# Kernel tuning notes

Measured on AMD Instinct MI355X. Metric: run time of the kernel, lower is better.

## Reference

```python
import jax, jax.numpy as jnp
import numpy as np

NG, ND = 50000, 10000          # gene / disease node counts
IN, HID = 64, 128              # in_feats / hidden_feats
EGG, EGD, EDG = 800000, 300000, 300000
EPS = 1e-5


def setup_inputs() -> dict:
    key = jax.random.key(0)
    ks = jax.random.split(key, 18)
    s = 0.05
    return {
        "xg": jax.random.normal(ks[0], (NG, IN), jnp.float32),
        "xd": jax.random.normal(ks[1], (ND, IN), jnp.float32),
        "Wn0": jax.random.normal(ks[2], (3, IN, HID), jnp.float32) * s,
        "Ws0": jax.random.normal(ks[3], (3, IN, HID), jnp.float32) * s,
        "b0": jnp.zeros((3, HID), jnp.float32),
        "Wn1": jax.random.normal(ks[4], (3, HID, HID), jnp.float32) * s,
        "Ws1": jax.random.normal(ks[5], (3, HID, HID), jnp.float32) * s,
        "b1": jnp.zeros((3, HID), jnp.float32),
        "bng": jnp.ones((2, 2, HID), jnp.float32),   # [layer, ntype, HID]
        "bnb": jnp.zeros((2, 2, HID), jnp.float32),
        "Wp": jax.random.normal(ks[6], (2, HID, IN), jnp.float32) * s,
        "bp": jnp.zeros((2, IN), jnp.float32),
        "gg_src": jax.random.randint(ks[7], (EGG,), 0, NG, jnp.int32),
        "gg_dst": jax.random.randint(ks[8], (EGG,), 0, NG, jnp.int32),
        "gd_src": jax.random.randint(ks[9], (EGD,), 0, NG, jnp.int32),
        "gd_dst": jax.random.randint(ks[10], (EGD,), 0, ND, jnp.int32),
        "dg_src": jax.random.randint(ks[11], (EDG,), 0, ND, jnp.int32),
        "dg_dst": jax.random.randint(ks[12], (EDG,), 0, NG, jnp.int32),
    }


def _seg_mean(h_src, src_idx, dst_idx, num_dst):
    # gather source features along edges, mean-reduce onto destinations
    msg = h_src[src_idx]                                         # [E, D]
    ssum = jax.ops.segment_sum(msg, dst_idx, num_segments=num_dst)
    deg = jax.ops.segment_sum(jnp.ones((dst_idx.shape[0], 1), h_src.dtype),
                              dst_idx, num_segments=num_dst)
    return ssum / jnp.maximum(deg, 1.0)                          # zero-degree -> 0


def _sage(h_src, h_dst, src_idx, dst_idx, num_dst, Wn, Ws, b):
    # DGL SAGEConv(mean): fc_neigh(mean_neigh) + fc_self(h_dst) + bias
    m = _seg_mean(h_src, src_idx, dst_idx, num_dst)
    return m @ Wn + h_dst @ Ws + b


def _bn_relu(x, g, b):
    # BatchNorm1d in training mode (batch statistics) followed by ReLU
    mu = x.mean(axis=0)
    var = x.var(axis=0)
    return jax.nn.relu((x - mu) * jax.lax.rsqrt(var + EPS) * g + b)


def _hetero_layer(hg, hd, Wn, Ws, b, idx):
    gg_s, gg_d, gd_s, gd_d, dg_s, dg_d = idx
    # HeteroGraphConv aggregate='sum' across relations per destination type
    out_g = (_sage(hg, hg, gg_s, gg_d, NG, Wn[0], Ws[0], b[0]) +
             _sage(hd, hg, dg_s, dg_d, NG, Wn[2], Ws[2], b[2]))
    out_d = _sage(hg, hd, gd_s, gd_d, ND, Wn[1], Ws[1], b[1])
    return out_g, out_d


def reference(xg, xd, Wn0, Ws0, b0, Wn1, Ws1, b1, bng, bnb, Wp, bp,
              gg_src, gg_dst, gd_src, gd_dst, dg_src, dg_dst):
    idx = (gg_src, gg_dst, gd_src, gd_dst, dg_src, dg_dst)
    # layer 0
    hg, hd = _hetero_layer(xg, xd, Wn0, Ws0, b0, idx)
    hg = _bn_relu(hg, bng[0, 0], bnb[0, 0])
    hd = _bn_relu(hd, bng[0, 1], bnb[0, 1])
    # layer 1
    hg, hd = _hetero_layer(hg, hd, Wn1, Ws1, b1, idx)
    hg = _bn_relu(hg, bng[1, 0], bnb[1, 0])
    hd = _bn_relu(hd, bng[1, 1], bnb[1, 1])
    # final per-type projection back to in_feats
    out_g = hg @ Wp[0] + bp[0]
    out_d = hd @ Wp[1] + bp[1]
    return out_g, out_d
```

## Files before the change

### kernel.cpp

```cpp
#include <hip/hip_runtime.h>

typedef unsigned short u16;
typedef __attribute__((ext_vector_type(8))) short bf16x8;
typedef __attribute__((ext_vector_type(4))) float f32x4;

__device__ __forceinline__ float BF(u16 u) { return __uint_as_float(((unsigned)u) << 16); }
__device__ __forceinline__ float BLO(unsigned p) { return __uint_as_float(p << 16); }
__device__ __forceinline__ float BHI(unsigned p) { return __uint_as_float(p & 0xffff0000u); }
__device__ __forceinline__ u16 FBF(float f) {
    unsigned u = __float_as_uint(f);
    u += 0x7FFFu + ((u >> 16) & 1u);
    return (u16)(u >> 16);
}
__device__ __forceinline__ unsigned PK2(float a, float b) {
    return (unsigned)FBF(a) | ((unsigned)FBF(b) << 16);
}
__device__ __forceinline__ float LD(const void* p, long i, int isf) {
    if (isf) return ((const float*)p)[i];
    return BF(((const u16*)p)[i]);
}

__global__ void HeteroGNN_78426102825755_kernel() {}

__global__ void hk_fill16(u16* p, long n, u16 v) {
    long i = (long)blockIdx.x * 256 + threadIdx.x;
    if (i < n) p[i] = v;
}
__global__ void hk_zeroi(int* p, int n) {
    int i = blockIdx.x * 256 + threadIdx.x;
    if (i < n) p[i] = 0;
}

__global__ void hk_detect(const void* x, int* flag) {
    __shared__ int cnt;
    if (threadIdx.x == 0) cnt = 0;
    __syncthreads();
    unsigned w = ((const unsigned*)x)[threadIdx.x];
    int e = (w >> 7) & 0xFF;
    int pl = (e >= 0x68 && e <= 0x92) ? 1 : 0;
    atomicAdd(&cnt, pl);
    __syncthreads();
    if (threadIdx.x == 0) flag[0] = (cnt >= 192) ? 0 : 1;
}

__device__ __forceinline__ void wprep_one(const void* W, int K, int ncol, int persh, int ksh,
                                          unsigned* dst, int i, int isf) {
    int mslice = i >> persh;
    int d2 = i & ((1 << persh) - 1);
    int mat = mslice >> ksh;
    int ks = mslice & ((1 << ksh) - 1);
    int ct = d2 >> 8; int rr = d2 & 255; int ln = rr >> 2; int j2 = rr & 3;
    int k1 = ks * 32 + ((ln >> 4) * 8 + 2 * j2);
    int n = ct * 16 + (ln & 15);
    long e = (long)mat * K * ncol + (long)k1 * ncol + n;
    dst[i] = PK2(LD(W, e, isf), LD(W, e + ncol, isf));
}
__device__ __forceinline__ void wsum_one(const void* W, int K, unsigned* dst, int i, int isf) {
    int ks = i >> 11; int d2 = i & 2047;
    int ct = d2 >> 8; int rr = d2 & 255; int ln = rr >> 2; int j2 = rr & 3;
    int k1 = ks * 32 + ((ln >> 4) * 8 + 2 * j2);
    int n = ct * 16 + (ln & 15);
    long e = (long)k1 * 128 + n;
    long e2 = e + (long)2 * K * 128;
    dst[i] = PK2(LD(W, e, isf) + LD(W, e2, isf), LD(W, e + 128, isf) + LD(W, e2 + 128, isf));
}

__global__ void hk_prep2(const void* Wn0, const void* Ws0, const void* Wn1, const void* Ws1,
                         unsigned* f0n, unsigned* f0s, unsigned* f1n, unsigned* f1s,
                         unsigned* f0sum, unsigned* f1sum,
                         const void* xg, const void* xd, long n0, long n1,
                         u16* og, u16* od, int* ncur, int Tn, int B1,
                         const int* dflag) {
    int isf = dflag[0];
    int b = blockIdx.x, t = threadIdx.x;
    if (b < 48)       { wprep_one(Wn0, 64, 128, 11, 1, f0n, b * 256 + t, isf); return; }
    if (b < 96)       { wprep_one(Ws0, 64, 128, 11, 1, f0s, (b - 48) * 256 + t, isf); return; }
    if (b < 192)      { wprep_one(Wn1, 128, 128, 11, 2, f1n, (b - 96) * 256 + t, isf); return; }
    if (b < 288)      { wprep_one(Ws1, 128, 128, 11, 2, f1s, (b - 192) * 256 + t, isf); return; }
    if (b < 304)      { wsum_one(Ws0, 64, f0sum, (b - 288) * 256 + t, isf); return; }
    if (b < 336)      { wsum_one(Ws1, 128, f1sum, (b - 304) * 256 + t, isf); return; }
    if (b < B1) {
        long i = (long)(b - 336) * 256 + t;
        if (i < n0) og[i] = FBF(LD(xg, i, isf));
        else if (i < n0 + n1) od[i - n0] = FBF(LD(xd, i - n0, isf));
        return;
    }
    int i = (b - B1) * 256 + t;
    if (i < Tn) ncur[i] = 0;
}

__global__ void hk_count3r(const int* d0, const int* d1, const int* d2,
                           int E0, int E1, int E2, int NGn, int* cnt, int* rank,
                           float* bnbuf) {
    int i = blockIdx.x * 256 + threadIdx.x;
    if (i < 512) bnbuf[i] = 0.f;
    int t;
    if (i < E0) t = d0[i];
    else if (i < E0 + E1) t = NGn + d1[i - E0];
    else if (i < E0 + E1 + E2) t = 2 * NGn + d2[i - E0 - E1];
    else return;
    rank[i] = atomicAdd(&cnt[t], 1);
}

__global__ void hk_count3(const int* d0, const int* d1, const int* d2,
                          int E0, int E1, int E2, int NGn, int* cnt) {
    int i = blockIdx.x * 256 + threadIdx.x;
    if (i < E0) atomicAdd(&cnt[d0[i]], 1);
    else if (i < E0 + E1) atomicAdd(&cnt[NGn + d1[i - E0]], 1);
    else if (i < E0 + E1 + E2) atomicAdd(&cnt[2 * NGn + d2[i - E0 - E1]], 1);
}

__global__ void hk_scan_a(const int* cnt, int n, int* pre, int* bsum) {
    __shared__ int lds[2048];
    __shared__ int part[256];
    int t = threadIdx.x;
    int base = blockIdx.x * 2048;
    for (int i = 0; i < 8; i++) {
        int idx = base + i * 256 + t;
        lds[i * 256 + t] = (idx < n) ? cnt[idx] : 0;
    }
    __syncthreads();
    int run[8];
    int s = 0;
    for (int i = 0; i < 8; i++) { run[i] = lds[t * 8 + i]; s += run[i]; }
    part[t] = s;
    __syncthreads();
    for (int o = 1; o < 256; o <<= 1) {
        int add = (t >= o) ? part[t - o] : 0;
        __syncthreads();
        part[t] += add;
        __syncthreads();
    }
    int ex = (t == 0) ? 0 : part[t - 1];
    for (int i = 0; i < 8; i++) {
        lds[t * 8 + i] = ex;
        ex += run[i];
    }
    __syncthreads();
    for (int i = 0; i < 8; i++) {
        int idx = base + i * 256 + t;
        if (idx < n) pre[idx] = lds[i * 256 + t];
    }
    if (t == 255) bsum[blockIdx.x] = part[255];
}

__global__ void hk_scan_b(int* bsum, int nb) {
    __shared__ int part[256];
    int t = threadIdx.x;
    part[t] = (t < nb) ? bsum[t] : 0;
    __syncthreads();
    for (int o = 1; o < 256; o <<= 1) {
        int add = (t >= o) ? part[t - o] : 0;
        __syncthreads();
        part[t] += add;
        __syncthreads();
    }
    if (t < nb) bsum[t] = (t == 0) ? 0 : part[t - 1];
    if (t == 0) bsum[nb] = part[nb - 1];
}

__global__ void hk_scan_c(const int* pre, const int* bsum, int n, int nb,
                          int* offs, int* cur) {
    int i = blockIdx.x * 256 + threadIdx.x;
    if (i < n) {
        int v = pre[i] + bsum[i >> 11];
        offs[i] = v;
        cur[i] = v;
    }
    if (i == 0) offs[n] = bsum[nb];
}

__global__ void hk_scatter3p(const int* s0, const int* d0, const int* s1, const int* d1,
                             const int* s2, const int* d2,
                             int E0, int E1, int E2, int NGn,
                             const int* offs, const int* rank, int* csr, float pscale) {
    int part = blockIdx.x & 7;
    int stride = (gridDim.x >> 3) * 256;
    int ET = E0 + E1 + E2;
    for (int i = (blockIdx.x >> 3) * 256 + threadIdx.x; i < ET; i += stride) {
        int t, s;
        if (i < E0) { t = d0[i]; s = s0[i]; }
        else if (i < E0 + E1) { int j = i - E0; t = NGn + d1[j]; s = s1[j]; }
        else { int j = i - E0 - E1; t = 2 * NGn + d2[j]; s = s2[j]; }
        int r = rank[i];
        int p = (int)((float)t * pscale);
        if (p > 7) p = 7;
        if (p == part) csr[offs[t] + r] = s;
    }
}

__global__ void hk_scatter3(const int* s0, const int* d0, const int* s1, const int* d1,
                            const int* s2, const int* d2,
                            int E0, int E1, int E2, int NGn, int* cur, int* csr,
                            float* bnbuf) {
    int i = blockIdx.x * 256 + threadIdx.x;
    if (i < 512) bnbuf[i] = 0.f;
    if (i < E0) { int p = atomicAdd(&cur[d0[i]], 1); csr[p] = s0[i]; }
    else if (i < E0 + E1) { int j = i - E0; int p = atomicAdd(&cur[NGn + d1[j]], 1); csr[p] = s1[j]; }
    else if (i < E0 + E1 + E2) { int j = i - E0 - E1; int p = atomicAdd(&cur[2 * NGn + d2[j]], 1); csr[p] = s2[j]; }
}

__device__ void mean64_rows(const unsigned* __restrict__ g, const int* __restrict__ offs,
                            const int* __restrict__ csr, unsigned* __restrict__ out,
                            int rA, int N, int lane) {
    int rB = rA + 1;
    if (rA >= N) return;
    int bA = offs[rA], eA = offs[rA + 1];
    int bB = 0, eB = 0;
    if (rB < N) { bB = offs[rB]; eB = offs[rB + 1]; }
    float sA0 = 0.f, sA1 = 0.f, sB0 = 0.f, sB1 = 0.f;
    int kA = bA, kB = bB;
    while (kA + 4 <= eA && kB + 4 <= eB) {
        unsigned pA0 = g[(long)csr[kA] * 64 + lane];
        unsigned pA1 = g[(long)csr[kA + 1] * 64 + lane];
        unsigned pA2 = g[(long)csr[kA + 2] * 64 + lane];
        unsigned pA3 = g[(long)csr[kA + 3] * 64 + lane];
        unsigned pB0 = g[(long)csr[kB] * 64 + lane];
        unsigned pB1 = g[(long)csr[kB + 1] * 64 + lane];
        unsigned pB2 = g[(long)csr[kB + 2] * 64 + lane];
        unsigned pB3 = g[(long)csr[kB + 3] * 64 + lane];
        sA0 += (BLO(pA0) + BLO(pA1)) + (BLO(pA2) + BLO(pA3));
        sA1 += (BHI(pA0) + BHI(pA1)) + (BHI(pA2) + BHI(pA3));
        sB0 += (BLO(pB0) + BLO(pB1)) + (BLO(pB2) + BLO(pB3));
        sB1 += (BHI(pB0) + BHI(pB1)) + (BHI(pB2) + BHI(pB3));
        kA += 4; kB += 4;
    }
    while (kA + 4 <= eA) {
        unsigned p0 = g[(long)csr[kA] * 64 + lane];
        unsigned p1 = g[(long)csr[kA + 1] * 64 + lane];
        unsigned p2 = g[(long)csr[kA + 2] * 64 + lane];
        unsigned p3 = g[(long)csr[kA + 3] * 64 + lane];
        sA0 += (BLO(p0) + BLO(p1)) + (BLO(p2) + BLO(p3));
        sA1 += (BHI(p0) + BHI(p1)) + (BHI(p2) + BHI(p3));
        kA += 4;
    }
    while (kB + 4 <= eB) {
        unsigned p0 = g[(long)csr[kB] * 64 + lane];
        unsigned p1 = g[(long)csr[kB + 1] * 64 + lane];
        unsigned p2 = g[(long)csr[kB + 2] * 64 + lane];
        unsigned p3 = g[(long)csr[kB + 3] * 64 + lane];
        sB0 += (BLO(p0) + BLO(p1)) + (BLO(p2) + BLO(p3));
        sB1 += (BHI(p0) + BHI(p1)) + (BHI(p2) + BHI(p3));
        kB += 4;
    }
    for (; kA < eA; kA++) {
        unsigned p = g[(long)csr[kA] * 64 + lane];
        sA0 += BLO(p); sA1 += BHI(p);
    }
    for (; kB < eB; kB++) {
        unsigned p = g[(long)csr[kB] * 64 + lane];
        sB0 += BLO(p); sB1 += BHI(p);
    }
    float invA = (eA > bA) ? 1.f / (float)(eA - bA) : 0.f;
    float invB = (eB > bB) ? 1.f / (float)(eB - bB) : 0.f;
    out[(long)rA * 64 + lane] = PK2(sA0 * invA, sA1 * invA);
    if (rB < N) out[(long)rB * 64 + lane] = PK2(sB0 * invB, sB1 * invB);
}

__device__ void mean32_rows(const unsigned* __restrict__ g, const int* __restrict__ offs,
                            const int* __restrict__ csr, unsigned* __restrict__ out,
                            int rA, int N, int l) {
    int rB = rA + 1;
    if (rA >= N) return;
    int bA = offs[rA], eA = offs[rA + 1];
    int bB = 0, eB = 0;
    if (rB < N) { bB = offs[rB]; eB = offs[rB + 1]; }
    float sA0 = 0.f, sA1 = 0.f, sB0 = 0.f, sB1 = 0.f;
    int kA = bA, kB = bB;
    while (kA + 4 <= eA && kB + 4 <= eB) {
        unsigned pA0 = g[(long)csr[kA] * 32 + l];
        unsigned pA1 = g[(long)csr[kA + 1] * 32 + l];
        unsigned pA2 = g[(long)csr[kA + 2] * 32 + l];
        unsigned pA3 = g[(long)csr[kA + 3] * 32 + l];
        unsigned pB0 = g[(long)csr[kB] * 32 + l];
        unsigned pB1 = g[(long)csr[kB + 1] * 32 + l];
        unsigned pB2 = g[(long)csr[kB + 2] * 32 + l];
        unsigned pB3 = g[(long)csr[kB + 3] * 32 + l];
        sA0 += (BLO(pA0) + BLO(pA1)) + (BLO(pA2) + BLO(pA3));
        sA1 += (BHI(pA0) + BHI(pA1)) + (BHI(pA2) + BHI(pA3));
        sB0 += (BLO(pB0) + BLO(pB1)) + (BLO(pB2) + BLO(pB3));
        sB1 += (BHI(pB0) + BHI(pB1)) + (BHI(pB2) + BHI(pB3));
        kA += 4; kB += 4;
    }
    while (kA + 4 <= eA) {
        unsigned p0 = g[(long)csr[kA] * 32 + l];
        unsigned p1 = g[(long)csr[kA + 1] * 32 + l];
        unsigned p2 = g[(long)csr[kA + 2] * 32 + l];
        unsigned p3 = g[(long)csr[kA + 3] * 32 + l];
        sA0 += (BLO(p0) + BLO(p1)) + (BLO(p2) + BLO(p3));
        sA1 += (BHI(p0) + BHI(p1)) + (BHI(p2) + BHI(p3));
        kA += 4;
    }
    while (kB + 4 <= eB) {
        unsigned p0 = g[(long)csr[kB] * 32 + l];
        unsigned p1 = g[(long)csr[kB + 1] * 32 + l];
        unsigned p2 = g[(long)csr[kB + 2] * 32 + l];
        unsigned p3 = g[(long)csr[kB + 3] * 32 + l];
        sB0 += (BLO(p0) + BLO(p1)) + (BLO(p2) + BLO(p3));
        sB1 += (BHI(p0) + BHI(p1)) + (BHI(p2) + BHI(p3));
        kB += 4;
    }
    for (; kA < eA; kA++) {
        unsigned p = g[(long)csr[kA] * 32 + l];
        sA0 += BLO(p); sA1 += BHI(p);
    }
    for (; kB < eB; kB++) {
        unsigned p = g[(long)csr[kB] * 32 + l];
        sB0 += BLO(p); sB1 += BHI(p);
    }
    float invA = (eA > bA) ? 1.f / (float)(eA - bA) : 0.f;
    float invB = (eB > bB) ? 1.f / (float)(eB - bB) : 0.f;
    out[(long)rA * 32 + l] = PK2(sA0 * invA, sA1 * invA);
    if (rB < N) out[(long)rB * 32 + l] = PK2(sB0 * invB, sB1 * invB);
}

__global__ void hk_mean32a(const unsigned* hg, const unsigned* hd,
                           const int* offs, const int* csr,
                           unsigned* mgg, unsigned* mdg, unsigned* mgd,
                           int NGn, int NDn, int nbg) {
    int b = blockIdx.x;
    const unsigned* g; const int* O; unsigned* o; int N; int rb;
    if (b < nbg)          { g = hg; O = offs;           o = mgg; N = NGn; rb = b * 16; }
    else if (b < 2 * nbg) { g = hd; O = offs + NGn;     o = mdg; N = NGn; rb = (b - nbg) * 16; }
    else                  { g = hg; O = offs + 2 * NGn; o = mgd; N = NDn; rb = (b - 2 * nbg) * 16; }
    int w = threadIdx.x >> 6, lane = threadIdx.x & 63;
    int half = lane >> 5, l = lane & 31;
    mean32_rows(g, O, csr, o, rb + w * 4 + half * 2, N, l);
}

__global__ void hk_mean64a(const unsigned* hg, const unsigned* hd,
                           const int* offs, const int* csr,
                           unsigned* mgg, unsigned* mdg, unsigned* mgd,
                           int NGn, int NDn, int nbg) {
    int b = blockIdx.x;
    const unsigned* g; const int* O; unsigned* o; int N; int rb;
    if (b < nbg)          { g = hg; O = offs;           o = mgg; N = NGn; rb = b * 8; }
    else if (b < 2 * nbg) { g = hd; O = offs + NGn;     o = mdg; N = NGn; rb = (b - nbg) * 8; }
    else                  { g = hg; O = offs + 2 * NGn; o = mgd; N = NDn; rb = (b - 2 * nbg) * 8; }
    int w = threadIdx.x >> 6, lane = threadIdx.x & 63;
    mean64_rows(g, O, csr, o, rb + w * 2, N, lane);
}

struct DS3 {
    const unsigned* AT[3];
    const unsigned* W[12];
    const void* bb; long b1off; long b2off;
    int N; u16* out; float* stats;
};

template<int NT, int KS, int RS, int PS>
__device__ __forceinline__ void ds3_body(const DS3& P, int row0, int isf,
                                         unsigned* lds, float* red) {
    constexpr int NS = NT * KS;
    int tid = threadIdx.x;
    int wave = tid >> 6, lane = tid & 63, m = lane & 15, quad = lane >> 4;
    bf16x8 B[NS];
#pragma unroll
    for (int s = 0; s < NS; s++)
        B[s] = *(const bf16x8*)(P.W[s] + wave * 256 + lane * 4);
    constexpr int R4 = RS / 4;
#pragma unroll
    for (int t = 0; t < NT; t++) {
        const uint4* src = (const uint4*)P.AT[t] + (long)row0 * R4;
#pragma unroll
        for (int j0 = 0; j0 < 64 * R4; j0 += 512) {
            int j = j0 + tid;
            int r = j / R4, c = j - r * R4;
            *(uint4*)&lds[(t * 64 + r) * PS + c * 4] = src[j];
        }
    }
    __syncthreads();

    f32x4 acc[4];
    f32x4 z = {0.f, 0.f, 0.f, 0.f};
#pragma unroll
    for (int rt = 0; rt < 4; rt++) acc[rt] = z;
#pragma unroll
    for (int s = 0; s < NS; s++) {
        const unsigned* ab = lds + (s / KS) * 64 * PS + (s % KS) * 16;
#pragma unroll
        for (int rt = 0; rt < 4; rt++) {
            bf16x8 af = *(const bf16x8*)(ab + (rt * 16 + m) * PS + quad * 4);
            acc[rt] = __builtin_amdgcn_mfma_f32_16x16x32_bf16(af, B[s], acc[rt], 0, 0, 0);
        }
    }
    if (tid < 256) red[tid] = 0.f;
    __syncthreads();
    int col = wave * 16 + m;
    float bv = LD(P.bb, P.b1off + col, isf);
    if (P.b2off >= 0) bv += LD(P.bb, P.b2off + col, isf);
    float ps = 0.f, ps2 = 0.f;
#pragma unroll
    for (int rt = 0; rt < 4; rt++) {
#pragma unroll
        for (int reg = 0; reg < 4; reg++) {
            int row = row0 + rt * 16 + quad * 4 + reg;
            if (row < P.N) {
                float v = acc[rt][reg] + bv;
                P.out[(long)row * 128 + col] = FBF(v);
                ps += v; ps2 += v * v;
            }
        }
    }
    atomicAdd(&red[col], ps);
    atomicAdd(&red[col + 128], ps2);
    __syncthreads();
    if (tid < 256) atomicAdd(&P.stats[tid], red[tid]);
}

template<int NTG, int NTD, int KS, int RS, int PS>
__global__ __launch_bounds__(512) void hk_dsage3(DS3 G, DS3 D, int gbl, const int* dflag) {
    __shared__ __align__(16) unsigned lds[NTG * 64 * PS];
    __shared__ float red[256];
    int isf = dflag[0];
    int b = blockIdx.x;
    if (b < gbl) ds3_body<NTG, KS, RS, PS>(G, b * 64, isf, lds, red);
    else         ds3_body<NTD, KS, RS, PS>(D, (b - gbl) * 64, isf, lds, red);
}

__device__ void hk_gath_bf(const unsigned* g, const int* offs, const int* csr,
                           unsigned* aTu, int wave, int lane, int row0, int N) {
    for (int i = 0; i < 8; i++) {
        int rA = wave * 16 + 2 * i, rB = rA + 1;
        int rowA = row0 + rA, rowB = row0 + rB;
        int bA = 0, eA = 0, bB = 0, eB = 0;
        if (rowA < N) { bA = offs[rowA]; eA = offs[rowA + 1]; }
        if (rowB < N) { bB = offs[rowB]; eB = offs[rowB + 1]; }
        float sA0 = 0.f, sA1 = 0.f, sB0 = 0.f, sB1 = 0.f;
        int kA = bA, kB = bB;
        for (; kA < eA; kA++) {
            unsigned p = g[(long)csr[kA] * 64 + lane];
            sA0 += BLO(p); sA1 += BHI(p);
        }
        for (; kB < eB; kB++) {
            unsigned p = g[(long)csr[kB] * 64 + lane];
            sB0 += BLO(p); sB1 += BHI(p);
        }
        float invA = (eA > bA) ? 1.f / (float)(eA - bA) : 0.f;
        float invB = (eB > bB) ? 1.f / (float)(eB - bB) : 0.f;
        aTu[rA * 68 + lane] = PK2(sA0 * invA, sA1 * invA);
        aTu[rB * 68 + lane] = PK2(sB0 * invB, sB1 * invB);
    }
}
__device__ void hk_gath64f(const float* g, const int* offs, const int* csr,
                           u16* aT16, int wave, int lane, int row0, int N) {
    for (int i = 0; i < 16; i++) {
        int r = wave * 16 + i, row = row0 + r;
        float s = 0.f, inv = 0.f;
        if (row < N) {
            int b = offs[row], e = offs[row + 1];
            for (int k = b; k < e; k++) s += g[(long)csr[k] * 64 + lane];
            if (e > b) inv = 1.f / (float)(e - b);
        }
        aT16[r * 80 + lane] = FBF(s * inv);
    }
}
__device__ void hk_gath64b(const u16* g, const int* offs, const int* csr,
                           u16* aT16, int wave, int lane, int row0, int N) {
    for (int i = 0; i < 16; i++) {
        int r = wave * 16 + i, row = row0 + r;
        float s = 0.f, inv = 0.f;
        if (row < N) {
            int b = offs[row], e = offs[row + 1];
            for (int k = b; k < e; k++) s += BF(g[(long)csr[k] * 64 + lane]);
            if (e > b) inv = 1.f / (float)(e - b);
        }
        aT16[r * 80 + lane] = FBF(s * inv);
    }
}

__device__ __forceinline__ void mfma_mat(const unsigned* Wf, int kslices,
                                         const unsigned* aTu, int strideU,
                                         unsigned* wsu, f32x4* accf,
                                         int tid, int wave, int lane) {
    int m = lane & 15, quad = lane >> 4;
    for (int ks = 0; ks < kslices; ks++) {
        const uint4* src = (const uint4*)(Wf + ks * 2048);
        uint4* dst = (uint4*)wsu;
        dst[tid] = src[tid];
        dst[tid + 256] = src[tid + 256];
        __syncthreads();
        bf16x8 af = *(const bf16x8*)(aTu + (wave * 16 + m) * strideU + ks * 16 + quad * 4);
        for (int ct = 0; ct < 8; ct++) {
            bf16x8 bf = *(const bf16x8*)(wsu + ct * 256 + lane * 4);
            accf[ct] = __builtin_amdgcn_mfma_f32_16x16x32_bf16(af, bf, accf[ct], 0, 0, 0);
        }
        __syncthreads();
    }
}

__device__ void hk_epilogue(f32x4* accf, const void* bb, long b1off, long b2off, int isf,
                            int N, int row0, u16* out, float* stats, float* red,
                            int tid, int wave, int lane) {
    int m = lane & 15, quad = lane >> 4;
    red[tid] = 0.f;
    __syncthreads();
    for (int ct = 0; ct < 8; ct++) {
        int col = ct * 16 + m;
        float bv = LD(bb, b1off + col, isf);
        if (b2off >= 0) bv += LD(bb, b2off + col, isf);
        float ps = 0.f, ps2 = 0.f;
        for (int reg = 0; reg < 4; reg++) {
            int row = row0 + wave * 16 + quad * 4 + reg;
            if (row < N) {
                float v = accf[ct][reg] + bv;
                out[(long)row * 128 + col] = FBF(v);
                ps += v; ps2 += v * v;
            }
        }
        atomicAdd(&red[col], ps);
        atomicAdd(&red[col + 128], ps2);
    }
    __syncthreads();
    if (tid < 128) {
        atomicAdd(&stats[tid], red[tid]);
        atomicAdd(&stats[tid + 128], red[tid + 128]);
    }
}

struct SageP {
    const void* h1; const int* off1; const int* csr1;
    const void* h2; const int* off2; const int* csr2;
    const void* hs;
    const unsigned* Wf1; const unsigned* Wf2;
    const unsigned* WfS1; const unsigned* WfS2;
    const void* bb; long b1off; long b2off;
    int N; u16* out; float* stats;
};

__global__ void hk_sage64m(SageP G, SageP D, int gb, const int* dflag) {
    __shared__ unsigned aTu[64 * 40];
    __shared__ unsigned wsu[2048];
    int gene = ((int)blockIdx.x < gb) ? 1 : 0;
    const SageP P = gene ? G : D;
    int isf = dflag[0];
    int tid = threadIdx.x;
    int wave = tid >> 6, lane = tid & 63;
    int row0 = (gene ? blockIdx.x : blockIdx.x - gb) * 64;
    u16* aT16 = (u16*)aTu;

    f32x4 z = {0.f, 0.f, 0.f, 0.f};
    f32x4 accf[8];
    for (int ct = 0; ct < 8; ct++) accf[ct] = z;

    if (isf) hk_gath64f((const float*)P.h1, P.off1, P.csr1, aT16, wave, lane, row0, P.N);
    else     hk_gath64b((const u16*)P.h1, P.off1, P.csr1, aT16, wave, lane, row0, P.N);
    __syncthreads();
    mfma_mat(P.Wf1, 2, aTu, 40, wsu, accf, tid, wave, lane);

    if (P.h2) {
        if (isf) hk_gath64f((const float*)P.h2, P.off2, P.csr2, aT16, wave, lane, row0, P.N);
        else     hk_gath64b((const u16*)P.h2, P.off2, P.csr2, aT16, wave, lane, row0, P.N);
        __syncthreads();
        mfma_mat(P.Wf2, 2, aTu, 40, wsu, accf, tid, wave, lane);
    }

    for (int i = 0; i < 16; i++) {
        int r = wave * 16 + i, row = row0 + r;
        aT16[r * 80 + lane] = (row < P.N) ? FBF(LD(P.hs, (long)row * 64 + lane, isf)) : (u16)0;
    }
    __syncthreads();
    mfma_mat(P.WfS1, 2, aTu, 40, wsu, accf, tid, wave, lane);
    if (P.WfS2) mfma_mat(P.WfS2, 2, aTu, 40, wsu, accf, tid, wave, lane);

    hk_epilogue(accf, P.bb, P.b1off, P.b2off, isf, P.N, row0, P.out, P.stats,
                (float*)wsu, tid, wave, lane);
}

__global__ void hk_sage128m(SageP G, SageP D, int gb, const int* dflag) {
    __shared__ unsigned aTu[64 * 68];
    __shared__ unsigned wsu[2048];
    int gene = ((int)blockIdx.x < gb) ? 1 : 0;
    const SageP P = gene ? G : D;
    int isf = dflag[0];
    int tid = threadIdx.x;
    int wave = tid >> 6, lane = tid & 63;
    int row0 = (gene ? blockIdx.x : blockIdx.x - gb) * 64;

    f32x4 z = {0.f, 0.f, 0.f, 0.f};
    f32x4 accf[8];
    for (int ct = 0; ct < 8; ct++) accf[ct] = z;

    hk_gath_bf((const unsigned*)P.h1, P.off1, P.csr1, aTu, wave, lane, row0, P.N);
    __syncthreads();
    mfma_mat(P.Wf1, 4, aTu, 68, wsu, accf, tid, wave, lane);

    if (P.h2) {
        hk_gath_bf((const unsigned*)P.h2, P.off2, P.csr2, aTu, wave, lane, row0, P.N);
        __syncthreads();
        mfma_mat(P.Wf2, 4, aTu, 68, wsu, accf, tid, wave, lane);
    }

    {
        const unsigned* gs = (const unsigned*)P.hs;
        for (int i = 0; i < 16; i++) {
            int r = wave * 16 + i, row = row0 + r;
            aTu[r * 68 + lane] = (row < P.N) ? gs[(long)row * 64 + lane] : 0u;
        }
        __syncthreads();
    }
    mfma_mat(P.WfS1, 4, aTu, 68, wsu, accf, tid, wave, lane);
    if (P.WfS2) mfma_mat(P.WfS2, 4, aTu, 68, wsu, accf, tid, wave, lane);

    hk_epilogue(accf, P.bb, P.b1off, P.b2off, isf, P.N, row0, P.out, P.stats,
                (float*)wsu, tid, wave, lane);
}

__global__ void hk_bnfinal2(float* buf, float invNg, float invNd,
                            const void* g, long gg, long gd,
                            const void* b, long bg, long bd, const int* dflag) {
    int isf = dflag[0];
    int t = threadIdx.x;
    int c = t & 127, isD = t >> 7;
    const float* st = buf + (isD ? 256 : 0);
    float invN = isD ? invNd : invNg;
    float mu = st[c] * invN;
    float var = st[c + 128] * invN - mu * mu;
    if (var < 0.f) var = 0.f;
    float sc = LD(g, (isD ? gd : gg) + c, isf) * rsqrtf(var + 1e-5f);
    float* o = buf + 512 + (isD ? 256 : 0);
    o[c] = sc;
    o[c + 128] = LD(b, (isD ? bd : bg) + c, isf) - mu * sc;
}

__global__ void hk_bnapply2(u16* xg_, long n8g, u16* xd_, long n8d, float* buf) {
    long i = (long)blockIdx.x * 256 + threadIdx.x;
    if (i < 512) buf[i] = 0.f;
    uint4* p; const float *sc, *sh; long k;
    if (i < n8g) { k = i; p = (uint4*)xg_; sc = buf + 512; sh = buf + 640; }
    else {
        k = i - n8g;
        if (k >= n8d) return;
        p = (uint4*)xd_; sc = buf + 768; sh = buf + 896;
    }
    uint4 v = p[k];
    int j = (int)(k & 15) * 8;
    float f[8] = {BLO(v.x), BHI(v.x), BLO(v.y), BHI(v.y),
                  BLO(v.z), BHI(v.z), BLO(v.w), BHI(v.w)};
    for (int c = 0; c < 8; c++) {
        float t = fmaf(f[c], sc[j + c], sh[j + c]);
        f[c] = (t > 0.f) ? t : 0.f;
    }
    uint4 o;
    o.x = PK2(f[0], f[1]); o.y = PK2(f[2], f[3]);
    o.z = PK2(f[4], f[5]); o.w = PK2(f[6], f[7]);
    p[k] = o;
}

__global__ void hk_proj2(const u16* Ag, int Ngn, const u16* Ad, int Ndn, int gbl,
                         const void* W, const void* bias, float* og, float* od,
                         const float* bn, const int* dflag) {
    const int S = 130;
    __shared__ float aT[64 * S];
    __shared__ float ws[2048];
    int isf = dflag[0];
    int tid = threadIdx.x;
    int gene = ((int)blockIdx.x < gbl) ? 1 : 0;
    const u16* A = gene ? Ag : Ad;
    int N = gene ? Ngn : Ndn;
    long woff = gene ? 0 : 8192;
    long boff = gene ? 0 : 64;
    float* out = gene ? og : od;
    const float* sc = bn + 512 + (gene ? 0 : 256);
    const float* sh = sc + 128;
    int wave = tid >> 6, lane = tid & 63;
    int jx = tid & 15, r0 = (tid >> 4) * 4;
    int row0 = (gene ? blockIdx.x : blockIdx.x - gbl) * 64;

    float2 scv = *(const float2*)&sc[2 * lane];
    float2 shv = *(const float2*)&sh[2 * lane];
    const unsigned* A32 = (const unsigned*)A;
    for (int i = 0; i < 16; i++) {
        int r = wave * 16 + i, row = row0 + r;
        unsigned p = (row < N) ? A32[(long)row * 64 + lane] : 0u;
        float2 v;
        v.x = fmaf(BLO(p), scv.x, shv.x); v.x = (v.x > 0.f) ? v.x : 0.f;
        v.y = fmaf(BHI(p), scv.y, shv.y); v.y = (v.y > 0.f) ? v.y : 0.f;
        *(float2*)&aT[r * S + 2 * lane] = v;
    }
    __syncthreads();

    float acc[4][4];
    for (int r = 0; r < 4; r++)
        for (int c = 0; c < 4; c++) acc[r][c] = 0.f;

    for (int k0 = 0; k0 < 128; k0 += 32) {
        for (int i = 0; i < 8; i++) {
            int idx = tid + i * 256;
            ws[idx] = LD(W, woff + (long)(k0 + (idx >> 6)) * 64 + (idx & 63), isf);
        }
        __syncthreads();
        for (int kk = 0; kk < 32; kk++) {
            float4 w4 = *(const float4*)(ws + kk * 64 + jx * 4);
            for (int r = 0; r < 4; r++) {
                float a = aT[(r0 + r) * S + k0 + kk];
                acc[r][0] = fmaf(a, w4.x, acc[r][0]);
                acc[r][1] = fmaf(a, w4.y, acc[r][1]);
                acc[r][2] = fmaf(a, w4.z, acc[r][2]);
                acc[r][3] = fmaf(a, w4.w, acc[r][3]);
            }
        }
        __syncthreads();
    }

    float b4[4];
    for (int c = 0; c < 4; c++) b4[c] = LD(bias, boff + jx * 4 + c, isf);
    for (int r = 0; r < 4; r++) {
        int row = row0 + r0 + r;
        if (row >= N) continue;
        float4 o;
        o.x = acc[r][0] + b4[0]; o.y = acc[r][1] + b4[1];
        o.z = acc[r][2] + b4[2]; o.w = acc[r][3] + b4[3];
        *(float4*)&out[(long)row * 64 + jx * 4] = o;
    }
}

__global__ void hk_proj(const u16* A, int N, const void* W, long woff,
                        const void* bias, long boff, float* out, const int* dflag) {
    const int S = 130;
    __shared__ float aT[64 * S];
    __shared__ float ws[2048];
    int isf = dflag[0];
    int tid = threadIdx.x;
    int wave = tid >> 6, lane = tid & 63;
    int jx = tid & 15, r0 = (tid >> 4) * 4;
    int row0 = blockIdx.x * 64;

    const unsigned* A32 = (const unsigned*)A;
    for (int i = 0; i < 16; i++) {
        int r = wave * 16 + i, row = row0 + r;
        unsigned p = (row < N) ? A32[(long)row * 64 + lane] : 0u;
        float2 v; v.x = BLO(p); v.y = BHI(p);
        *(float2*)&aT[r * S + 2 * lane] = v;
    }
    __syncthreads();

    float acc[4][4];
    for (int r = 0; r < 4; r++)
        for (int c = 0; c < 4; c++) acc[r][c] = 0.f;

    for (int k0 = 0; k0 < 128; k0 += 32) {
        for (int i = 0; i < 8; i++) {
            int idx = tid + i * 256;
            ws[idx] = LD(W, woff + (long)(k0 + (idx >> 6)) * 64 + (idx & 63), isf);
        }
        __syncthreads();
        for (int kk = 0; kk < 32; kk++) {
            float4 w4 = *(const float4*)(ws + kk * 64 + jx * 4);
            for (int r = 0; r < 4; r++) {
                float a = aT[(r0 + r) * S + k0 + kk];
                acc[r][0] = fmaf(a, w4.x, acc[r][0]);
                acc[r][1] = fmaf(a, w4.y, acc[r][1]);
                acc[r][2] = fmaf(a, w4.z, acc[r][2]);
                acc[r][3] = fmaf(a, w4.w, acc[r][3]);
            }
        }
        __syncthreads();
    }

    float b4[4];
    for (int c = 0; c < 4; c++) b4[c] = LD(bias, boff + jx * 4 + c, isf);
    for (int r = 0; r < 4; r++) {
        int row = row0 + r0 + r;
        if (row >= N) continue;
        float4 o;
        o.x = acc[r][0] + b4[0]; o.y = acc[r][1] + b4[1];
        o.z = acc[r][2] + b4[2]; o.w = acc[r][3] + b4[3];
        *(float4*)&out[(long)row * 64 + jx * 4] = o;
    }
}

extern "C" void kernel_launch(void* const* d_in, const int* in_sizes, int n_in,
                              void* d_out, int out_size, void* d_ws, size_t ws_size,
                              hipStream_t stream) {
    const void* xg = d_in[0];
    const void* xd = d_in[1];
    const void* Wn0 = d_in[2];
    const void* Ws0 = d_in[3];
    const void* b0 = d_in[4];
    const void* Wn1 = d_in[5];
    const void* Ws1 = d_in[6];
    const void* b1 = d_in[7];
    const void* bng = d_in[8];
    const void* bnb = d_in[9];
    const void* Wp = d_in[10];
    const void* bp = d_in[11];
    const int* gg_src = (const int*)d_in[12];
    const int* gg_dst = (const int*)d_in[13];
    const int* gd_src = (const int*)d_in[14];
    const int* gd_dst = (const int*)d_in[15];
    const int* dg_src = (const int*)d_in[16];
    const int* dg_dst = (const int*)d_in[17];

    const int NG = in_sizes[0] / 64;
    const int ND = in_sizes[1] / 64;
    const int EGG = in_sizes[12];
    const int EGD = in_sizes[14];
    const int EDG = in_sizes[16];

    const int NGp = (NG + 63) & ~63;
    const int NDp = (ND + 63) & ~63;
    const int Tn = 2 * NG + ND;
    const int ET = EGG + EDG + EGD;

    float* outf = (float*)d_out;

    char* base = (char*)d_ws;
    size_t off = 0;
    u16* hg0; u16* pg1;
    unsigned *wf0n, *wf0s, *wf1n, *wf1s, *wf0sum, *wf1sum;
    int *csr, *offs, *ncur, *scanpre, *scanbs;
    int* dflag;
    float* bnbuf;
    {
        hg0 = (u16*)(base + off);      off += (size_t)NGp * 128 * 2; off = (off + 255) & ~(size_t)255;
        pg1 = (u16*)(base + off);      off += (size_t)NGp * 128 * 2; off = (off + 255) & ~(size_t)255;
        wf0n = (unsigned*)(base + off); off += 3 * 4096 * 4;         off = (off + 255) & ~(size_t)255;
        wf0s = (unsigned*)(base + off); off += 3 * 4096 * 4;         off = (off + 255) & ~(size_t)255;
        wf1n = (unsigned*)(base + off); off += 3 * 8192 * 4;         off = (off + 255) & ~(size_t)255;
        wf1s = (unsigned*)(base + off); off += 3 * 8192 * 4;         off = (off + 255) & ~(size_t)255;
        wf0sum = (unsigned*)(base + off); off += 4096 * 4;           off = (off + 255) & ~(size_t)255;
        wf1sum = (unsigned*)(base + off); off += 8192 * 4;           off = (off + 255) & ~(size_t)255;
        csr = (int*)(base + off);      off += (size_t)ET * 4;        off = (off + 255) & ~(size_t)255;
        offs = (int*)(base + off);     off += (size_t)(Tn + 1) * 4;  off = (off + 255) & ~(size_t)255;
        ncur = (int*)(base + off);     off += (size_t)Tn * 4;        off = (off + 255) & ~(size_t)255;
        scanpre = (int*)(base + off);  off += (size_t)Tn * 4;        off = (off + 255) & ~(size_t)255;
        scanbs = (int*)(base + off);   off += 257 * 4;               off = (off + 255) & ~(size_t)255;
        bnbuf = (float*)(base + off);  off += 1024 * 4;              off = (off + 255) & ~(size_t)255;
        dflag = (int*)(base + off);    off += 256;                   off = (off + 255) & ~(size_t)255;
    }
    size_t off_base = off;
    unsigned* meanP = (unsigned*)(base + off); off += (size_t)NGp * 128 * 4; off = (off + 255) & ~(size_t)255;
    size_t off_mean = off;
    u16* pd1ws = (u16*)(base + off); off += (size_t)NDp * 128 * 2;
    size_t off_full = off;

    int tier;
    if (off_full <= ws_size) tier = 2;
    else if (off_mean <= ws_size) tier = 1;
    else if (off_base <= ws_size) tier = 0;
    else {
        hk_fill16<<<(int)(((long)out_size * 2 + 255) / 256), 256, 0, stream>>>(
            (u16*)d_out, (long)out_size * 2, (u16)0x4000);
        return;
    }

    u16* hd0 = (u16*)d_out;
    u16* pd1out = hd0 + (long)NDp * 128;
    unsigned* mgdM = (unsigned*)(pd1out + (long)NDp * 128);

    u16* xg16 = pg1;
    u16* xd16 = pg1 + (long)NGp * 64;

    hk_detect<<<1, 256, 0, stream>>>(xg, dflag);
    {
        int B1 = 336 + (int)(((long)(NG + ND) * 64 + 255) / 256);
        int B2 = B1 + (Tn + 255) / 256;
        hk_prep2<<<B2, 256, 0, stream>>>(Wn0, Ws0, Wn1, Ws1,
                                         wf0n, wf0s, wf1n, wf1s, wf0sum, wf1sum,
                                         xg, xd, (long)NG * 64, (long)ND * 64,
                                         xg16, xd16, ncur, Tn, B1, dflag);
    }

    const int gb = NGp / 64, db = NDp / 64;

    if (tier >= 1) {
        int* rank = (int*)meanP;
        hk_count3r<<<(ET + 255) / 256, 256, 0, stream>>>(gg_dst, dg_dst, gd_dst,
                                                         EGG, EDG, EGD, NG, ncur, rank, bnbuf);
        {
            int nbT = (Tn + 2047) / 2048;
            hk_scan_a<<<nbT, 256, 0, stream>>>(ncur, Tn, scanpre, scanbs);
            hk_scan_b<<<1, 256, 0, stream>>>(scanbs, nbT);
            hk_scan_c<<<(Tn + 255) / 256, 256, 0, stream>>>(scanpre, scanbs, Tn, nbT, offs, ncur);
        }
        hk_scatter3p<<<8 * 208, 256, 0, stream>>>(gg_src, gg_dst, dg_src, dg_dst,
                                                  gd_src, gd_dst, EGG, EDG, EGD,
                                                  NG, offs, rank, csr, 8.0f / (float)Tn);
    } else {
        hk_count3<<<(ET + 255) / 256, 256, 0, stream>>>(gg_dst, dg_dst, gd_dst,
                                                        EGG, EDG, EGD, NG, ncur);
        {
            int nbT = (Tn + 2047) / 2048;
            hk_scan_a<<<nbT, 256, 0, stream>>>(ncur, Tn, scanpre, scanbs);
            hk_scan_b<<<1, 256, 0, stream>>>(scanbs, nbT);
            hk_scan_c<<<(Tn + 255) / 256, 256, 0, stream>>>(scanpre, scanbs, Tn, nbT, offs, ncur);
        }
        hk_scatter3<<<(ET + 255) / 256, 256, 0, stream>>>(gg_src, gg_dst, dg_src, dg_dst,
                                                          gd_src, gd_dst, EGG, EDG, EGD,
                                                          NG, ncur, csr, bnbuf);
    }

    if (tier >= 1) {
        unsigned* xg16u = (unsigned*)xg16;
        unsigned* xd16u = (unsigned*)xd16;
        unsigned* hg0u = (unsigned*)hg0;
        unsigned* hd0u = (unsigned*)hd0;
        unsigned* mggM = meanP;
        unsigned* mdg0 = meanP + (long)NGp * 32;
        unsigned* mdg1 = meanP + (long)NGp * 64;
        u16* pd1 = (tier == 2) ? pd1ws : pd1out;

        DS3 G = {}, D = {};

        {
            int nbg = (NG + 15) / 16, nbd = (ND + 15) / 16;
            hk_mean32a<<<2 * nbg + nbd, 256, 0, stream>>>(xg16u, xd16u, offs, csr,
                                                          mggM, mdg0, mgdM, NG, ND, nbg);
        }
        G.AT[0] = mggM;  G.W[0] = wf0n;             G.W[1] = wf0n + 2048;
        G.AT[1] = mdg0;  G.W[2] = wf0n + 2 * 4096;  G.W[3] = wf0n + 2 * 4096 + 2048;
        G.AT[2] = xg16u; G.W[4] = wf0sum;           G.W[5] = wf0sum + 2048;
        G.bb = b0; G.b1off = 0; G.b2off = 256;
        G.N = NG; G.out = hg0; G.stats = bnbuf;
        D.AT[0] = mgdM;  D.W[0] = wf0n + 4096;      D.W[1] = wf0n + 4096 + 2048;
        D.AT[1] = xd16u; D.W[2] = wf0s + 4096;      D.W[3] = wf0s + 4096 + 2048;
        D.bb = b0; D.b1off = 128; D.b2off = -1;
        D.N = ND; D.out = hd0; D.stats = bnbuf + 256;
        hk_dsage3<3, 2, 2, 32, 36><<<gb + db, 512, 0, stream>>>(G, D, gb, dflag);
        hk_bnfinal2<<<1, 256, 0, stream>>>(bnbuf, 1.f / NG, 1.f / ND, bng, 0L, 128L, bnb, 0L, 128L, dflag);
        hk_bnapply2<<<(int)(((long)(NG + ND) * 16 + 255) / 256), 256, 0, stream>>>(
            hg0, (long)NG * 16, hd0, (long)ND * 16, bnbuf);

        {
            int nbg = (NG + 7) / 8, nbd = (ND + 7) / 8;
            hk_mean64a<<<2 * nbg + nbd, 256, 0, stream>>>(hg0u, hd0u, offs, csr,
                                                          mggM, mdg1, mgdM, NG, ND, nbg);
        }
        G = DS3{}; D = DS3{};
        G.AT[0] = mggM;  G.AT[1] = mdg1;  G.AT[2] = hg0u;
        D.AT[0] = mgdM;  D.AT[1] = hd0u;
        for (int ks = 0; ks < 4; ks++) {
            G.W[ks] = wf1n + ks * 2048;
            G.W[4 + ks] = wf1n + 2 * 8192 + ks * 2048;
            G.W[8 + ks] = wf1sum + ks * 2048;
            D.W[ks] = wf1n + 8192 + ks * 2048;
            D.W[4 + ks] = wf1s + 8192 + ks * 2048;
        }
        G.bb = b1; G.b1off = 0; G.b2off = 256;
        G.N = NG; G.out = pg1; G.stats = bnbuf;
        D.bb = b1; D.b1off = 128; D.b2off = -1;
        D.N = ND; D.out = pd1; D.stats = bnbuf + 256;
        hk_dsage3<3, 2, 4, 64, 68><<<gb + db, 512, 0, stream>>>(G, D, gb, dflag);
        hk_bnfinal2<<<1, 256, 0, stream>>>(bnbuf, 1.f / NG, 1.f / ND, bng, 256L, 384L, bnb, 256L, 384L, dflag);

        if (tier == 2) {
            hk_proj2<<<gb + db, 256, 0, stream>>>(pg1, NG, pd1, ND, gb, Wp, bp,
                                                  outf, outf + (long)NG * 64, bnbuf, dflag);
        } else {
            hk_proj2<<<db, 256, 0, stream>>>(pg1, NG, pd1, ND, 0, Wp, bp,
                                             outf, outf + (long)NG * 64, bnbuf, dflag);
            hk_proj2<<<gb, 256, 0, stream>>>(pg1, NG, pd1, ND, gb, Wp, bp,
                                             outf, outf + (long)NG * 64, bnbuf, dflag);
        }
    } else {
        SageP G, D;

        G.h1 = xg; G.off1 = offs;          G.csr1 = csr;
        G.h2 = xd; G.off2 = offs + NG;     G.csr2 = csr;
        G.hs = xg;
        G.Wf1 = wf0n; G.Wf2 = wf0n + 2 * 4096;
        G.WfS1 = wf0s; G.WfS2 = wf0s + 2 * 4096;
        G.bb = b0; G.b1off = 0; G.b2off = 256;
        G.N = NG; G.out = hg0; G.stats = bnbuf;
        D.h1 = xg; D.off1 = offs + 2 * NG; D.csr1 = csr;
        D.h2 = 0; D.off2 = 0; D.csr2 = 0;
        D.hs = xd;
        D.Wf1 = wf0n + 4096; D.Wf2 = 0;
        D.WfS1 = wf0s + 4096; D.WfS2 = 0;
        D.bb = b0; D.b1off = 128; D.b2off = -1;
        D.N = ND; D.out = hd0; D.stats = bnbuf + 256;
        hk_sage64m<<<gb + db, 256, 0, stream>>>(G, D, gb, dflag);
        hk_bnfinal2<<<1, 256, 0, stream>>>(bnbuf, 1.f / NG, 1.f / ND, bng, 0L, 128L, bnb, 0L, 128L, dflag);
        hk_bnapply2<<<(int)(((long)(NG + ND) * 16 + 255) / 256), 256, 0, stream>>>(
            hg0, (long)NG * 16, hd0, (long)ND * 16, bnbuf);

        G.h1 = hg0; G.off1 = offs;          G.csr1 = csr;
        G.h2 = hd0; G.off2 = offs + NG;     G.csr2 = csr;
        G.hs = hg0;
        G.Wf1 = wf1n; G.Wf2 = wf1n + 2 * 8192;
        G.WfS1 = wf1s; G.WfS2 = wf1s + 2 * 8192;
        G.bb = b1; G.b1off = 0; G.b2off = 256;
        G.N = NG; G.out = pg1; G.stats = bnbuf;
        D.h1 = hg0; D.off1 = offs + 2 * NG; D.csr1 = csr;
        D.h2 = 0; D.off2 = 0; D.csr2 = 0;
        D.hs = hd0;
        D.Wf1 = wf1n + 8192; D.Wf2 = 0;
        D.WfS1 = wf1s + 8192; D.WfS2 = 0;
        D.bb = b1; D.b1off = 128; D.b2off = -1;
        D.N = ND; D.out = pd1out; D.stats = bnbuf + 256;
        hk_sage128m<<<gb + db, 256, 0, stream>>>(G, D, gb, dflag);
        hk_bnfinal2<<<1, 256, 0, stream>>>(bnbuf, 1.f / NG, 1.f / ND, bng, 256L, 384L, bnb, 256L, 384L, dflag);
        hk_bnapply2<<<(int)(((long)(NG + ND) * 16 + 255) / 256), 256, 0, stream>>>(
            pg1, (long)NG * 16, pd1out, (long)ND * 16, bnbuf);

        hk_proj<<<db, 256, 0, stream>>>(pd1out, ND, Wp, 8192L, bp, 64L, outf + (long)NG * 64, dflag);
        hk_proj<<<gb, 256, 0, stream>>>(pg1, NG, Wp, 0L, bp, 0L, outf, dflag);
    }
}
```

Measured before the change: 426.0 us.

## Fuse neighbor mean gather and BN apply into SAGE matmul kernel

Removes the separate mean-aggregation kernels and the BN-apply pass. The fused SAGE kernel now gathers neighbor features straight into LDS and applies the previous layer's BN+ReLU on the fly while gathering and staging self features. It also merges edge counting into the weight-prep kernel and folds the zero-init into the detect kernel, which cuts launches and drops the old fallback tiers. This avoids writing and re-reading the intermediate mean buffers. In exchange each block does irregular gathers inside the matmul kernel, which may lower occupancy or weaken latency hiding.

```diff
diff --git a/kernel.cpp b/kernel.cpp
--- a/kernel.cpp
+++ b/kernel.cpp
@@ -26,21 +26,21 @@
     long i = (long)blockIdx.x * 256 + threadIdx.x;
     if (i < n) p[i] = v;
 }
-__global__ void hk_zeroi(int* p, int n) {
+
+__global__ void hk_detect2(const void* x, int* flag, int* ncur, int Tn, float* bnbuf) {
     int i = blockIdx.x * 256 + threadIdx.x;
-    if (i < n) p[i] = 0;
-}
-
-__global__ void hk_detect(const void* x, int* flag) {
-    __shared__ int cnt;
-    if (threadIdx.x == 0) cnt = 0;
-    __syncthreads();
-    unsigned w = ((const unsigned*)x)[threadIdx.x];
-    int e = (w >> 7) & 0xFF;
-    int pl = (e >= 0x68 && e <= 0x92) ? 1 : 0;
-    atomicAdd(&cnt, pl);
-    __syncthreads();
-    if (threadIdx.x == 0) flag[0] = (cnt >= 192) ? 0 : 1;
+    if (i < Tn) ncur[i] = 0;
+    if (i < 512) bnbuf[i] = 0.f;
+    if (blockIdx.x == 0) {
+        __shared__ int cnt;
+        if (threadIdx.x == 0) cnt = 0;
+        __syncthreads();
+        unsigned w = ((const unsigned*)x)[threadIdx.x];
+        int e = (w >> 7) & 0xFF;
+        atomicAdd(&cnt, (e >= 0x68 && e <= 0x92) ? 1 : 0);
+        __syncthreads();
+        if (threadIdx.x == 0) flag[0] = (cnt >= 192) ? 0 : 1;
+    }
 }
 
 __device__ __forceinline__ void wprep_one(const void* W, int K, int ncol, int persh, int ksh,
@@ -65,49 +65,36 @@
     dst[i] = PK2(LD(W, e, isf) + LD(W, e2, isf), LD(W, e + 128, isf) + LD(W, e2 + 128, isf));
 }
 
-__global__ void hk_prep2(const void* Wn0, const void* Ws0, const void* Wn1, const void* Ws1,
-                         unsigned* f0n, unsigned* f0s, unsigned* f1n, unsigned* f1s,
-                         unsigned* f0sum, unsigned* f1sum,
-                         const void* xg, const void* xd, long n0, long n1,
-                         u16* og, u16* od, int* ncur, int Tn, int B1,
-                         const int* dflag) {
+__global__ void hk_prepcnt(const void* Wn0, const void* Ws0, const void* Wn1, const void* Ws1,
+                           unsigned* f0n, unsigned* f0s, unsigned* f1n, unsigned* f1s,
+                           unsigned* f0sum, unsigned* f1sum,
+                           const void* xg, const void* xd, long n0, long n1,
+                           u16* og, u16* od, int Cb,
+                           const int* d0, const int* d1, const int* d2,
+                           int E0, int E1, int E2, int NGn, int* cnt, int* rank,
+                           const int* dflag) {
+    int b = blockIdx.x, t = threadIdx.x;
+    if (b < Cb) {
+        int i = b * 256 + t;
+        int tn;
+        if (i < E0) tn = d0[i];
+        else if (i < E0 + E1) tn = NGn + d1[i - E0];
+        else if (i < E0 + E1 + E2) tn = 2 * NGn + d2[i - E0 - E1];
+        else return;
+        rank[i] = atomicAdd(&cnt[tn], 1);
+        return;
+    }
     int isf = dflag[0];
-    int b = blockIdx.x, t = threadIdx.x;
-    if (b < 48)       { wprep_one(Wn0, 64, 128, 11, 1, f0n, b * 256 + t, isf); return; }
-    if (b < 96)       { wprep_one(Ws0, 64, 128, 11, 1, f0s, (b - 48) * 256 + t, isf); return; }
-    if (b < 192)      { wprep_one(Wn1, 128, 128, 11, 2, f1n, (b - 96) * 256 + t, isf); return; }
-    if (b < 288)      { wprep_one(Ws1, 128, 128, 11, 2, f1s, (b - 192) * 256 + t, isf); return; }
-    if (b < 304)      { wsum_one(Ws0, 64, f0sum, (b - 288) * 256 + t, isf); return; }
-    if (b < 336)      { wsum_one(Ws1, 128, f1sum, (b - 304) * 256 + t, isf); return; }
-    if (b < B1) {
-        long i = (long)(b - 336) * 256 + t;
-        if (i < n0) og[i] = FBF(LD(xg, i, isf));
-        else if (i < n0 + n1) od[i - n0] = FBF(LD(xd, i - n0, isf));
-        return;
-    }
-    int i = (b - B1) * 256 + t;
-    if (i < Tn) ncur[i] = 0;
-}
-
-__global__ void hk_count3r(const int* d0, const int* d1, const int* d2,
-                           int E0, int E1, int E2, int NGn, int* cnt, int* rank,
-                           float* bnbuf) {
-    int i = blockIdx.x * 256 + threadIdx.x;
-    if (i < 512) bnbuf[i] = 0.f;
-    int t;
-    if (i < E0) t = d0[i];
-    else if (i < E0 + E1) t = NGn + d1[i - E0];
-    else if (i < E0 + E1 + E2) t = 2 * NGn + d2[i - E0 - E1];
-    else return;
-    rank[i] = atomicAdd(&cnt[t], 1);
-}
-
-__global__ void hk_count3(const int* d0, const int* d1, const int* d2,
-                          int E0, int E1, int E2, int NGn, int* cnt) {
-    int i = blockIdx.x * 256 + threadIdx.x;
-    if (i < E0) atomicAdd(&cnt[d0[i]], 1);
-    else if (i < E0 + E1) atomicAdd(&cnt[NGn + d1[i - E0]], 1);
-    else if (i < E0 + E1 + E2) atomicAdd(&cnt[2 * NGn + d2[i - E0 - E1]], 1);
+    b -= Cb;
+    if (b < 48)  { wprep_one(Wn0, 64, 128, 11, 1, f0n, b * 256 + t, isf); return; }
+    if (b < 96)  { wprep_one(Ws0, 64, 128, 11, 1, f0s, (b - 48) * 256 + t, isf); return; }
+    if (b < 192) { wprep_one(Wn1, 128, 128, 11, 2, f1n, (b - 96) * 256 + t, isf); return; }
+    if (b < 288) { wprep_one(Ws1, 128, 128, 11, 2, f1s, (b - 192) * 256 + t, isf); return; }
+    if (b < 304) { wsum_one(Ws0, 64, f0sum, (b - 288) * 256 + t, isf); return; }
+    if (b < 336) { wsum_one(Ws1, 128, f1sum, (b - 304) * 256 + t, isf); return; }
+    long i = (long)(b - 336) * 256 + t;
+    if (i < n0) og[i] = FBF(LD(xg, i, isf));
+    else if (i < n0 + n1) od[i - n0] = FBF(LD(xd, i - n0, isf));
 }
 
 __global__ void hk_scan_a(const int* cnt, int n, int* pre, int* bsum) {
@@ -159,14 +146,9 @@
     if (t == 0) bsum[nb] = part[nb - 1];
 }
 
-__global__ void hk_scan_c(const int* pre, const int* bsum, int n, int nb,
-                          int* offs, int* cur) {
+__global__ void hk_scan_c(const int* pre, const int* bsum, int n, int nb, int* offs) {
     int i = blockIdx.x * 256 + threadIdx.x;
-    if (i < n) {
-        int v = pre[i] + bsum[i >> 11];
-        offs[i] = v;
-        cur[i] = v;
-    }
+    if (i < n) offs[i] = pre[i] + bsum[i >> 11];
     if (i == 0) offs[n] = bsum[nb];
 }
 
@@ -178,37 +160,48 @@
     int stride = (gridDim.x >> 3) * 256;
     int ET = E0 + E1 + E2;
     for (int i = (blockIdx.x >> 3) * 256 + threadIdx.x; i < ET; i += stride) {
-        int t, s;
-        if (i < E0) { t = d0[i]; s = s0[i]; }
-        else if (i < E0 + E1) { int j = i - E0; t = NGn + d1[j]; s = s1[j]; }
-        else { int j = i - E0 - E1; t = 2 * NGn + d2[j]; s = s2[j]; }
-        int r = rank[i];
+        int t;
+        if (i < E0) t = d0[i];
+        else if (i < E0 + E1) t = NGn + d1[i - E0];
+        else t = 2 * NGn + d2[i - E0 - E1];
         int p = (int)((float)t * pscale);
         if (p > 7) p = 7;
-        if (p == part) csr[offs[t] + r] = s;
-    }
-}
-
-__global__ void hk_scatter3(const int* s0, const int* d0, const int* s1, const int* d1,
-                            const int* s2, const int* d2,
-                            int E0, int E1, int E2, int NGn, int* cur, int* csr,
-                            float* bnbuf) {
-    int i = blockIdx.x * 256 + threadIdx.x;
-    if (i < 512) bnbuf[i] = 0.f;
-    if (i < E0) { int p = atomicAdd(&cur[d0[i]], 1); csr[p] = s0[i]; }
-    else if (i < E0 + E1) { int j = i - E0; int p = atomicAdd(&cur[NGn + d1[j]], 1); csr[p] = s1[j]; }
-    else if (i < E0 + E1 + E2) { int j = i - E0 - E1; int p = atomicAdd(&cur[2 * NGn + d2[j]], 1); csr[p] = s2[j]; }
-}
-
-__device__ void mean64_rows(const unsigned* __restrict__ g, const int* __restrict__ offs,
-                            const int* __restrict__ csr, unsigned* __restrict__ out,
-                            int rA, int N, int lane) {
-    int rB = rA + 1;
-    if (rA >= N) return;
-    int bA = offs[rA], eA = offs[rA + 1];
+        if (p != part) continue;
+        int s = (i < E0) ? s0[i] : (i < E0 + E1) ? s1[i - E0] : s2[i - E0 - E1];
+        csr[offs[t] + rank[i]] = s;
+    }
+}
+
+struct FS {
+    const unsigned* gsrc[2]; const int* goffs[2]; const float* gbn[2];
+    const unsigned* ssrc; const float* sbn;
+    const int* csr;
+    const unsigned* W[12];
+    const void* bb; long b1off; long b2off;
+    int N; u16* out; float* stats;
+};
+
+template<bool BN>
+__device__ void m64row(const unsigned* __restrict__ g, const int* __restrict__ offs,
+                       const int* __restrict__ csr, unsigned* __restrict__ lds, int PSl,
+                       int r, int row0, int N, int lane, const float* __restrict__ bn) {
+    int gA = row0 + r, gB = gA + 1;
+    if (gA >= N) return;
+    int bA = offs[gA], eA = offs[gA + 1];
     int bB = 0, eB = 0;
-    if (rB < N) { bB = offs[rB]; eB = offs[rB + 1]; }
+    if (gB < N) { bB = offs[gB]; eB = offs[gB + 1]; }
+    float scx = 0.f, scy = 0.f, shx = 0.f, shy = 0.f;
+    if (BN) {
+        float2 s2 = *(const float2*)&bn[2 * lane];
+        float2 h2 = *(const float2*)&bn[128 + 2 * lane];
+        scx = s2.x; scy = s2.y; shx = h2.x; shy = h2.y;
+    }
     float sA0 = 0.f, sA1 = 0.f, sB0 = 0.f, sB1 = 0.f;
+    auto ACC = [&](unsigned p, float& s0, float& s1) {
+        float vx = BLO(p), vy = BHI(p);
+        if (BN) { vx = fmaxf(fmaf(vx, scx, shx), 0.f); vy = fmaxf(fmaf(vy, scy, shy), 0.f); }
+        s0 += vx; s1 += vy;
+    };
     int kA = bA, kB = bB;
     while (kA + 4 <= eA && kB + 4 <= eB) {
         unsigned pA0 = g[(long)csr[kA] * 64 + lane];
@@ -219,10 +212,8 @@
         unsigned pB1 = g[(long)csr[kB + 1] * 64 + lane];
         unsigned pB2 = g[(long)csr[kB + 2] * 64 + lane];
         unsigned pB3 = g[(long)csr[kB + 3] * 64 + lane];
-        sA0 += (BLO(pA0) + BLO(pA1)) + (BLO(pA2) + BLO(pA3));
-        sA1 += (BHI(pA0) + BHI(pA1)) + (BHI(pA2) + BHI(pA3));
-        sB0 += (BLO(pB0) + BLO(pB1)) + (BLO(pB2) + BLO(pB3));
-        sB1 += (BHI(pB0) + BHI(pB1)) + (BHI(pB2) + BHI(pB3));
+        ACC(pA0, sA0, sA1); ACC(pA1, sA0, sA1); ACC(pA2, sA0, sA1); ACC(pA3, sA0, sA1);
+        ACC(pB0, sB0, sB1); ACC(pB1, sB0, sB1); ACC(pB2, sB0, sB1); ACC(pB3, sB0, sB1);
         kA += 4; kB += 4;
     }
     while (kA + 4 <= eA) {
@@ -230,8 +221,7 @@
         unsigned p1 = g[(long)csr[kA + 1] * 64 + lane];
         unsigned p2 = g[(long)csr[kA + 2] * 64 + lane];
         unsigned p3 = g[(long)csr[kA + 3] * 64 + lane];
-        sA0 += (BLO(p0) + BLO(p1)) + (BLO(p2) + BLO(p3));
-        sA1 += (BHI(p0) + BHI(p1)) + (BHI(p2) + BHI(p3));
+        ACC(p0, sA0, sA1); ACC(p1, sA0, sA1); ACC(p2, sA0, sA1); ACC(p3, sA0, sA1);
         kA += 4;
     }
     while (kB + 4 <= eB) {
@@ -239,32 +229,25 @@
         unsigned p1 = g[(long)csr[kB + 1] * 64 + lane];
         unsigned p2 = g[(long)csr[kB + 2] * 64 + lane];
         unsigned p3 = g[(long)csr[kB + 3] * 64 + lane];
-        sB0 += (BLO(p0) + BLO(p1)) + (BLO(p2) + BLO(p3));
-        sB1 += (BHI(p0) + BHI(p1)) + (BHI(p2) + BHI(p3));
+        ACC(p0, sB0, sB1); ACC(p1, sB0, sB1); ACC(p2, sB0, sB1); ACC(p3, sB0, sB1);
         kB += 4;
     }
-    for (; kA < eA; kA++) {
-        unsigned p = g[(long)csr[kA] * 64 + lane];
-        sA0 += BLO(p); sA1 += BHI(p);
-    }
-    for (; kB < eB; kB++) {
-        unsigned p = g[(long)csr[kB] * 64 + lane];
-        sB0 += BLO(p); sB1 += BHI(p);
-    }
+    for (; kA < eA; kA++) { unsigned p = g[(long)csr[kA] * 64 + lane]; ACC(p, sA0, sA1); }
+    for (; kB < eB; kB++) { unsigned p = g[(long)csr[kB] * 64 + lane]; ACC(p, sB0, sB1); }
     float invA = (eA > bA) ? 1.f / (float)(eA - bA) : 0.f;
     float invB = (eB > bB) ? 1.f / (float)(eB - bB) : 0.f;
-    out[(long)rA * 64 + lane] = PK2(sA0 * invA, sA1 * invA);
-    if (rB < N) out[(long)rB * 64 + lane] = PK2(sB0 * invB, sB1 * invB);
-}
-
-__device__ void mean32_rows(const unsigned* __restrict__ g, const int* __restrict__ offs,
-                            const int* __restrict__ csr, unsigned* __restrict__ out,
-                            int rA, int N, int l) {
-    int rB = rA + 1;
-    if (rA >= N) return;
-    int bA = offs[rA], eA = offs[rA + 1];
+    lds[r * PSl + lane] = PK2(sA0 * invA, sA1 * invA);
+    if (gB < N) lds[(r + 1) * PSl + lane] = PK2(sB0 * invB, sB1 * invB);
+}
+
+__device__ void m32row(const unsigned* __restrict__ g, const int* __restrict__ offs,
+                       const int* __restrict__ csr, unsigned* __restrict__ lds, int PSl,
+                       int r, int row0, int N, int l) {
+    int gA = row0 + r, gB = gA + 1;
+    if (gA >= N) return;
+    int bA = offs[gA], eA = offs[gA + 1];
     int bB = 0, eB = 0;
-    if (rB < N) { bB = offs[rB]; eB = offs[rB + 1]; }
+    if (gB < N) { bB = offs[gB]; eB = offs[gB + 1]; }
     float sA0 = 0.f, sA1 = 0.f, sB0 = 0.f, sB1 = 0.f;
     int kA = bA, kB = bB;
     while (kA + 4 <= eA && kB + 4 <= eB) {
@@ -310,65 +293,62 @@
     }
     float invA = (eA > bA) ? 1.f / (float)(eA - bA) : 0.f;
     float invB = (eB > bB) ? 1.f / (float)(eB - bB) : 0.f;
-    out[(long)rA * 32 + l] = PK2(sA0 * invA, sA1 * invA);
-    if (rB < N) out[(long)rB * 32 + l] = PK2(sB0 * invB, sB1 * invB);
-}
-
-__global__ void hk_mean32a(const unsigned* hg, const unsigned* hd,
-                           const int* offs, const int* csr,
-                           unsigned* mgg, unsigned* mdg, unsigned* mgd,
-                           int NGn, int NDn, int nbg) {
-    int b = blockIdx.x;
-    const unsigned* g; const int* O; unsigned* o; int N; int rb;
-    if (b < nbg)          { g = hg; O = offs;           o = mgg; N = NGn; rb = b * 16; }
-    else if (b < 2 * nbg) { g = hd; O = offs + NGn;     o = mdg; N = NGn; rb = (b - nbg) * 16; }
-    else                  { g = hg; O = offs + 2 * NGn; o = mgd; N = NDn; rb = (b - 2 * nbg) * 16; }
-    int w = threadIdx.x >> 6, lane = threadIdx.x & 63;
-    int half = lane >> 5, l = lane & 31;
-    mean32_rows(g, O, csr, o, rb + w * 4 + half * 2, N, l);
-}
-
-__global__ void hk_mean64a(const unsigned* hg, const unsigned* hd,
-                           const int* offs, const int* csr,
-                           unsigned* mgg, unsigned* mdg, unsigned* mgd,
-                           int NGn, int NDn, int nbg) {
-    int b = blockIdx.x;
-    const unsigned* g; const int* O; unsigned* o; int N; int rb;
-    if (b < nbg)          { g = hg; O = offs;           o = mgg; N = NGn; rb = b * 8; }
-    else if (b < 2 * nbg) { g = hd; O = offs + NGn;     o = mdg; N = NGn; rb = (b - nbg) * 8; }
-    else                  { g = hg; O = offs + 2 * NGn; o = mgd; N = NDn; rb = (b - 2 * nbg) * 8; }
-    int w = threadIdx.x >> 6, lane = threadIdx.x & 63;
-    mean64_rows(g, O, csr, o, rb + w * 2, N, lane);
-}
-
-struct DS3 {
-    const unsigned* AT[3];
-    const unsigned* W[12];
-    const void* bb; long b1off; long b2off;
-    int N; u16* out; float* stats;
-};
-
-template<int NT, int KS, int RS, int PS>
-__device__ __forceinline__ void ds3_body(const DS3& P, int row0, int isf,
-                                         unsigned* lds, float* red) {
-    constexpr int NS = NT * KS;
+    lds[r * PSl + l] = PK2(sA0 * invA, sA1 * invA);
+    if (gB < N) lds[(r + 1) * PSl + l] = PK2(sB0 * invB, sB1 * invB);
+}
+
+template<int NM, int RS, int PS, bool BN>
+__device__ __forceinline__ void stage_self(const FS& P, int row0, unsigned* lds, int tid) {
+    constexpr int R4 = RS / 4;
+    const uint4* src = (const uint4*)P.ssrc + (long)row0 * R4;
+#pragma unroll
+    for (int j0 = 0; j0 < 64 * R4; j0 += 512) {
+        int j = j0 + tid;
+        int r = j / R4, c = j - r * R4;
+        uint4 v = src[j];
+        if (BN) {
+            unsigned w[4] = {v.x, v.y, v.z, v.w};
+#pragma unroll
+            for (int q = 0; q < 4; q++) {
+                int col = 8 * c + 2 * q;
+                float2 s2 = *(const float2*)&P.sbn[col];
+                float2 h2 = *(const float2*)&P.sbn[128 + col];
+                w[q] = PK2(fmaxf(fmaf(BLO(w[q]), s2.x, h2.x), 0.f),
+                           fmaxf(fmaf(BHI(w[q]), s2.y, h2.y), 0.f));
+            }
+            v.x = w[0]; v.y = w[1]; v.z = w[2]; v.w = w[3];
+        }
+        *(uint4*)&lds[(NM * 64 + r) * PS + c * 4] = v;
+    }
+}
+
+template<int NM, int KS, int RS, int PS, bool BN>
+__device__ __forceinline__ void fs_body(const FS& P, int row0, int isf,
+                                        unsigned* lds, float* red) {
+    constexpr int NS = (NM + 1) * KS;
     int tid = threadIdx.x;
     int wave = tid >> 6, lane = tid & 63, m = lane & 15, quad = lane >> 4;
     bf16x8 B[NS];
 #pragma unroll
     for (int s = 0; s < NS; s++)
         B[s] = *(const bf16x8*)(P.W[s] + wave * 256 + lane * 4);
-    constexpr int R4 = RS / 4;
-#pragma unroll
-    for (int t = 0; t < NT; t++) {
-        const uint4* src = (const uint4*)P.AT[t] + (long)row0 * R4;
-#pragma unroll
-        for (int j0 = 0; j0 < 64 * R4; j0 += 512) {
-            int j = j0 + tid;
-            int r = j / R4, c = j - r * R4;
-            *(uint4*)&lds[(t * 64 + r) * PS + c * 4] = src[j];
+#pragma unroll
+    for (int t = 0; t < NM; t++) {
+        unsigned* lt = lds + t * 64 * PS;
+        if constexpr (RS == 64) {
+#pragma unroll
+            for (int p = 0; p < 4; p++)
+                m64row<BN>(P.gsrc[t], P.goffs[t], P.csr, lt, PS,
+                           wave * 8 + 2 * p, row0, P.N, lane, P.gbn[t]);
+        } else {
+            int half = lane >> 5, l = lane & 31;
+#pragma unroll
+            for (int p = 0; p < 2; p++)
+                m32row(P.gsrc[t], P.goffs[t], P.csr, lt, PS,
+                       wave * 8 + 4 * p + 2 * half, row0, P.N, l);
         }
     }
+    stage_self<NM, RS, PS, BN>(P, row0, lds, tid);
     __syncthreads();
 
     f32x4 acc[4];
@@ -408,202 +388,14 @@
     if (tid < 256) atomicAdd(&P.stats[tid], red[tid]);
 }
 
-template<int NTG, int NTD, int KS, int RS, int PS>
-__global__ __launch_bounds__(512) void hk_dsage3(DS3 G, DS3 D, int gbl, const int* dflag) {
-    __shared__ __align__(16) unsigned lds[NTG * 64 * PS];
+template<int NMG, int NMD, int KS, int RS, int PS, bool BN>
+__global__ __launch_bounds__(512) void hk_fsage(FS G, FS D, int gbl, const int* dflag) {
+    __shared__ __align__(16) unsigned lds[(NMG + 1) * 64 * PS];
     __shared__ float red[256];
     int isf = dflag[0];
     int b = blockIdx.x;
-    if (b < gbl) ds3_body<NTG, KS, RS, PS>(G, b * 64, isf, lds, red);
-    else         ds3_body<NTD, KS, RS, PS>(D, (b - gbl) * 64, isf, lds, red);
-}
-
-__device__ void hk_gath_bf(const unsigned* g, const int* offs, const int* csr,
-                           unsigned* aTu, int wave, int lane, int row0, int N) {
-    for (int i = 0; i < 8; i++) {
-        int rA = wave * 16 + 2 * i, rB = rA + 1;
-        int rowA = row0 + rA, rowB = row0 + rB;
-        int bA = 0, eA = 0, bB = 0, eB = 0;
-        if (rowA < N) { bA = offs[rowA]; eA = offs[rowA + 1]; }
-        if (rowB < N) { bB = offs[rowB]; eB = offs[rowB + 1]; }
-        float sA0 = 0.f, sA1 = 0.f, sB0 = 0.f, sB1 = 0.f;
-        int kA = bA, kB = bB;
-        for (; kA < eA; kA++) {
-            unsigned p = g[(long)csr[kA] * 64 + lane];
-            sA0 += BLO(p); sA1 += BHI(p);
-        }
-        for (; kB < eB; kB++) {
-            unsigned p = g[(long)csr[kB] * 64 + lane];
-            sB0 += BLO(p); sB1 += BHI(p);
-        }
-        float invA = (eA > bA) ? 1.f / (float)(eA - bA) : 0.f;
-        float invB = (eB > bB) ? 1.f / (float)(eB - bB) : 0.f;
-        aTu[rA * 68 + lane] = PK2(sA0 * invA, sA1 * invA);
-        aTu[rB * 68 + lane] = PK2(sB0 * invB, sB1 * invB);
-    }
-}
-__device__ void hk_gath64f(const float* g, const int* offs, const int* csr,
-                           u16* aT16, int wave, int lane, int row0, int N) {
-    for (int i = 0; i < 16; i++) {
-        int r = wave * 16 + i, row = row0 + r;
-        float s = 0.f, inv = 0.f;
-        if (row < N) {
-            int b = offs[row], e = offs[row + 1];
-            for (int k = b; k < e; k++) s += g[(long)csr[k] * 64 + lane];
-            if (e > b) inv = 1.f / (float)(e - b);
-        }
-        aT16[r * 80 + lane] = FBF(s * inv);
-    }
-}
-__device__ void hk_gath64b(const u16* g, const int* offs, const int* csr,
-                           u16* aT16, int wave, int lane, int row0, int N) {
-    for (int i = 0; i < 16; i++) {
-        int r = wave * 16 + i, row = row0 + r;
-        float s = 0.f, inv = 0.f;
-        if (row < N) {
-            int b = offs[row], e = offs[row + 1];
-            for (int k = b; k < e; k++) s += BF(g[(long)csr[k] * 64 + lane]);
-            if (e > b) inv = 1.f / (float)(e - b);
-        }
-        aT16[r * 80 + lane] = FBF(s * inv);
-    }
-}
-
-__device__ __forceinline__ void mfma_mat(const unsigned* Wf, int kslices,
-                                         const unsigned* aTu, int strideU,
-                                         unsigned* wsu, f32x4* accf,
-                                         int tid, int wave, int lane) {
-    int m = lane & 15, quad = lane >> 4;
-    for (int ks = 0; ks < kslices; ks++) {
-        const uint4* src = (const uint4*)(Wf + ks * 2048);
-        uint4* dst = (uint4*)wsu;
-        dst[tid] = src[tid];
-        dst[tid + 256] = src[tid + 256];
-        __syncthreads();
-        bf16x8 af = *(const bf16x8*)(aTu + (wave * 16 + m) * strideU + ks * 16 + quad * 4);
-        for (int ct = 0; ct < 8; ct++) {
-            bf16x8 bf = *(const bf16x8*)(wsu + ct * 256 + lane * 4);
-            accf[ct] = __builtin_amdgcn_mfma_f32_16x16x32_bf16(af, bf, accf[ct], 0, 0, 0);
-        }
-        __syncthreads();
-    }
-}
-
-__device__ void hk_epilogue(f32x4* accf, const void* bb, long b1off, long b2off, int isf,
-                            int N, int row0, u16* out, float* stats, float* red,
-                            int tid, int wave, int lane) {
-    int m = lane & 15, quad = lane >> 4;
-    red[tid] = 0.f;
-    __syncthreads();
-    for (int ct = 0; ct < 8; ct++) {
-        int col = ct * 16 + m;
-        float bv = LD(bb, b1off + col, isf);
-        if (b2off >= 0) bv += LD(bb, b2off + col, isf);
-        float ps = 0.f, ps2 = 0.f;
-        for (int reg = 0; reg < 4; reg++) {
-            int row = row0 + wave * 16 + quad * 4 + reg;
-            if (row < N) {
-                float v = accf[ct][reg] + bv;
-                out[(long)row * 128 + col] = FBF(v);
-                ps += v; ps2 += v * v;
-            }
-        }
-        atomicAdd(&red[col], ps);
-        atomicAdd(&red[col + 128], ps2);
-    }
-    __syncthreads();
-    if (tid < 128) {
-        atomicAdd(&stats[tid], red[tid]);
-        atomicAdd(&stats[tid + 128], red[tid + 128]);
-    }
-}
-
-struct SageP {
-    const void* h1; const int* off1; const int* csr1;
-    const void* h2; const int* off2; const int* csr2;
-    const void* hs;
-    const unsigned* Wf1; const unsigned* Wf2;
-    const unsigned* WfS1; const unsigned* WfS2;
-    const void* bb; long b1off; long b2off;
-    int N; u16* out; float* stats;
-};
-
-__global__ void hk_sage64m(SageP G, SageP D, int gb, const int* dflag) {
-    __shared__ unsigned aTu[64 * 40];
-    __shared__ unsigned wsu[2048];
-    int gene = ((int)blockIdx.x < gb) ? 1 : 0;
-    const SageP P = gene ? G : D;
-    int isf = dflag[0];
-    int tid = threadIdx.x;
-    int wave = tid >> 6, lane = tid & 63;
-    int row0 = (gene ? blockIdx.x : blockIdx.x - gb) * 64;
-    u16* aT16 = (u16*)aTu;
-
-    f32x4 z = {0.f, 0.f, 0.f, 0.f};
-    f32x4 accf[8];
-    for (int ct = 0; ct < 8; ct++) accf[ct] = z;
-
-    if (isf) hk_gath64f((const float*)P.h1, P.off1, P.csr1, aT16, wave, lane, row0, P.N);
-    else     hk_gath64b((const u16*)P.h1, P.off1, P.csr1, aT16, wave, lane, row0, P.N);
-    __syncthreads();
-    mfma_mat(P.Wf1, 2, aTu, 40, wsu, accf, tid, wave, lane);
-
-    if (P.h2) {
-        if (isf) hk_gath64f((const float*)P.h2, P.off2, P.csr2, aT16, wave, lane, row0, P.N);
-        else     hk_gath64b((const u16*)P.h2, P.off2, P.csr2, aT16, wave, lane, row0, P.N);
-        __syncthreads();
-        mfma_mat(P.Wf2, 2, aTu, 40, wsu, accf, tid, wave, lane);
-    }
-
-    for (int i = 0; i < 16; i++) {
-        int r = wave * 16 + i, row = row0 + r;
-        aT16[r * 80 + lane] = (row < P.N) ? FBF(LD(P.hs, (long)row * 64 + lane, isf)) : (u16)0;
-    }
-    __syncthreads();
-    mfma_mat(P.WfS1, 2, aTu, 40, wsu, accf, tid, wave, lane);
-    if (P.WfS2) mfma_mat(P.WfS2, 2, aTu, 40, wsu, accf, tid, wave, lane);
-
-    hk_epilogue(accf, P.bb, P.b1off, P.b2off, isf, P.N, row0, P.out, P.stats,
-                (float*)wsu, tid, wave, lane);
-}
-
-__global__ void hk_sage128m(SageP G, SageP D, int gb, const int* dflag) {
-    __shared__ unsigned aTu[64 * 68];
-    __shared__ unsigned wsu[2048];
-    int gene = ((int)blockIdx.x < gb) ? 1 : 0;
-    const SageP P = gene ? G : D;
-    int isf = dflag[0];
-    int tid = threadIdx.x;
-    int wave = tid >> 6, lane = tid & 63;
-    int row0 = (gene ? blockIdx.x : blockIdx.x - gb) * 64;
-
-    f32x4 z = {0.f, 0.f, 0.f, 0.f};
-    f32x4 accf[8];
-    for (int ct = 0; ct < 8; ct++) accf[ct] = z;
-
-    hk_gath_bf((const unsigned*)P.h1, P.off1, P.csr1, aTu, wave, lane, row0, P.N);
-    __syncthreads();
-    mfma_mat(P.Wf1, 4, aTu, 68, wsu, accf, tid, wave, lane);
-
-    if (P.h2) {
-        hk_gath_bf((const unsigned*)P.h2, P.off2, P.csr2, aTu, wave, lane, row0, P.N);
-        __syncthreads();
-        mfma_mat(P.Wf2, 4, aTu, 68, wsu, accf, tid, wave, lane);
-    }
-
-    {
-        const unsigned* gs = (const unsigned*)P.hs;
-        for (int i = 0; i < 16; i++) {
-            int r = wave * 16 + i, row = row0 + r;
-            aTu[r * 68 + lane] = (row < P.N) ? gs[(long)row * 64 + lane] : 0u;
-        }
-        __syncthreads();
-    }
-    mfma_mat(P.WfS1, 4, aTu, 68, wsu, accf, tid, wave, lane);
-    if (P.WfS2) mfma_mat(P.WfS2, 4, aTu, 68, wsu, accf, tid, wave, lane);
-
-    hk_epilogue(accf, P.bb, P.b1off, P.b2off, isf, P.N, row0, P.out, P.stats,
-                (float*)wsu, tid, wave, lane);
+    if (b < gbl) fs_body<NMG, KS, RS, PS, BN>(G, b * 64, isf, lds, red);
+    else         fs_body<NMD, KS, RS, PS, BN>(D, (b - gbl) * 64, isf, lds, red);
 }
 
 __global__ void hk_bnfinal2(float* buf, float invNg, float invNd,
@@ -612,39 +404,18 @@
     int isf = dflag[0];
     int t = threadIdx.x;
     int c = t & 127, isD = t >> 7;
-    const float* st = buf + (isD ? 256 : 0);
+    float* st = buf + (isD ? 256 : 0);
     float invN = isD ? invNd : invNg;
-    float mu = st[c] * invN;
-    float var = st[c + 128] * invN - mu * mu;
+    float s1 = st[c], s2 = st[c + 128];
+    float mu = s1 * invN;
+    float var = s2 * invN - mu * mu;
     if (var < 0.f) var = 0.f;
     float sc = LD(g, (isD ? gd : gg) + c, isf) * rsqrtf(var + 1e-5f);
     float* o = buf + 512 + (isD ? 256 : 0);
     o[c] = sc;
     o[c + 128] = LD(b, (isD ? bd : bg) + c, isf) - mu * sc;
-}
-
-__global__ void hk_bnapply2(u16* xg_, long n8g, u16* xd_, long n8d, float* buf) {
-    long i = (long)blockIdx.x * 256 + threadIdx.x;
-    if (i < 512) buf[i] = 0.f;
-    uint4* p; const float *sc, *sh; long k;
-    if (i < n8g) { k = i; p = (uint4*)xg_; sc = buf + 512; sh = buf + 640; }
-    else {
-        k = i - n8g;
-        if (k >= n8d) return;
-        p = (uint4*)xd_; sc = buf + 768; sh = buf + 896;
-    }
-    uint4 v = p[k];
-    int j = (int)(k & 15) * 8;
-    float f[8] = {BLO(v.x), BHI(v.x), BLO(v.y), BHI(v.y),
-                  BLO(v.z), BHI(v.z), BLO(v.w), BHI(v.w)};
-    for (int c = 0; c < 8; c++) {
-        float t = fmaf(f[c], sc[j + c], sh[j + c]);
-        f[c] = (t > 0.f) ? t : 0.f;
-    }
-    uint4 o;
-    o.x = PK2(f[0], f[1]); o.y = PK2(f[2], f[3]);
-    o.z = PK2(f[4], f[5]); o.w = PK2(f[6], f[7]);
-    p[k] = o;
+    st[c] = 0.f;
+    st[c + 128] = 0.f;
 }
 
 __global__ void hk_proj2(const u16* Ag, int Ngn, const u16* Ad, int Ndn, int gbl,
@@ -676,61 +447,6 @@
         float2 v;
         v.x = fmaf(BLO(p), scv.x, shv.x); v.x = (v.x > 0.f) ? v.x : 0.f;
         v.y = fmaf(BHI(p), scv.y, shv.y); v.y = (v.y > 0.f) ? v.y : 0.f;
-        *(float2*)&aT[r * S + 2 * lane] = v;
-    }
-    __syncthreads();
-
-    float acc[4][4];
-    for (int r = 0; r < 4; r++)
-        for (int c = 0; c < 4; c++) acc[r][c] = 0.f;
-
-    for (int k0 = 0; k0 < 128; k0 += 32) {
-        for (int i = 0; i < 8; i++) {
-            int idx = tid + i * 256;
-            ws[idx] = LD(W, woff + (long)(k0 + (idx >> 6)) * 64 + (idx & 63), isf);
-        }
-        __syncthreads();
-        for (int kk = 0; kk < 32; kk++) {
-            float4 w4 = *(const float4*)(ws + kk * 64 + jx * 4);
-            for (int r = 0; r < 4; r++) {
-                float a = aT[(r0 + r) * S + k0 + kk];
-                acc[r][0] = fmaf(a, w4.x, acc[r][0]);
-                acc[r][1] = fmaf(a, w4.y, acc[r][1]);
-                acc[r][2] = fmaf(a, w4.z, acc[r][2]);
-                acc[r][3] = fmaf(a, w4.w, acc[r][3]);
-            }
-        }
-        __syncthreads();
-    }
-
-    float b4[4];
-    for (int c = 0; c < 4; c++) b4[c] = LD(bias, boff + jx * 4 + c, isf);
-    for (int r = 0; r < 4; r++) {
-        int row = row0 + r0 + r;
-        if (row >= N) continue;
-        float4 o;
-        o.x = acc[r][0] + b4[0]; o.y = acc[r][1] + b4[1];
-        o.z = acc[r][2] + b4[2]; o.w = acc[r][3] + b4[3];
-        *(float4*)&out[(long)row * 64 + jx * 4] = o;
-    }
-}
-
-__global__ void hk_proj(const u16* A, int N, const void* W, long woff,
-                        const void* bias, long boff, float* out, const int* dflag) {
-    const int S = 130;
-    __shared__ float aT[64 * S];
-    __shared__ float ws[2048];
-    int isf = dflag[0];
-    int tid = threadIdx.x;
-    int wave = tid >> 6, lane = tid & 63;
-    int jx = tid & 15, r0 = (tid >> 4) * 4;
-    int row0 = blockIdx.x * 64;
-
-    const unsigned* A32 = (const unsigned*)A;
-    for (int i = 0; i < 16; i++) {
-        int r = wave * 16 + i, row = row0 + r;
-        unsigned p = (row < N) ? A32[(long)row * 64 + lane] : 0u;
-        float2 v; v.x = BLO(p); v.y = BHI(p);
         *(float2*)&aT[r * S + 2 * lane] = v;
     }
     __syncthreads();
@@ -830,15 +546,12 @@
         dflag = (int*)(base + off);    off += 256;                   off = (off + 255) & ~(size_t)255;
     }
     size_t off_base = off;
-    unsigned* meanP = (unsigned*)(base + off); off += (size_t)NGp * 128 * 4; off = (off + 255) & ~(size_t)255;
-    size_t off_mean = off;
     u16* pd1ws = (u16*)(base + off); off += (size_t)NDp * 128 * 2;
     size_t off_full = off;
 
     int tier;
     if (off_full <= ws_size) tier = 2;
-    else if (off_mean <= ws_size) tier = 1;
-    else if (off_base <= ws_size) tier = 0;
+    else if (off_base <= ws_size) tier = 1;
     else {
         hk_fill16<<<(int)(((long)out_size * 2 + 255) / 256), 256, 0, stream>>>(
             (u16*)d_out, (long)out_size * 2, (u16)0x4000);
@@ -847,154 +560,88 @@
 
     u16* hd0 = (u16*)d_out;
     u16* pd1out = hd0 + (long)NDp * 128;
-    unsigned* mgdM = (unsigned*)(pd1out + (long)NDp * 128);
+    u16* pd1 = (tier == 2) ? pd1ws : pd1out;
 
     u16* xg16 = pg1;
     u16* xd16 = pg1 + (long)NGp * 64;
-
-    hk_detect<<<1, 256, 0, stream>>>(xg, dflag);
+    int* rank = (int*)hg0;
+
+    hk_detect2<<<(Tn + 255) / 256, 256, 0, stream>>>(xg, dflag, ncur, Tn, bnbuf);
+
     {
-        int B1 = 336 + (int)(((long)(NG + ND) * 64 + 255) / 256);
-        int B2 = B1 + (Tn + 255) / 256;
-        hk_prep2<<<B2, 256, 0, stream>>>(Wn0, Ws0, Wn1, Ws1,
-                                         wf0n, wf0s, wf1n, wf1s, wf0sum, wf1sum,
-                                         xg, xd, (long)NG * 64, (long)ND * 64,
-                                         xg16, xd16, ncur, Tn, B1, dflag);
-    }
+        int Cb = (ET + 255) / 256;
+        int Tb = (int)(((long)(NG + ND) * 64 + 255) / 256);
+        hk_prepcnt<<<Cb + 336 + Tb, 256, 0, stream>>>(
+            Wn0, Ws0, Wn1, Ws1, wf0n, wf0s, wf1n, wf1s, wf0sum, wf1sum,
+            xg, xd, (long)NG * 64, (long)ND * 64, xg16, xd16, Cb,
+            gg_dst, dg_dst, gd_dst, EGG, EDG, EGD, NG, ncur, rank, dflag);
+    }
+
+    {
+        int nbT = (Tn + 2047) / 2048;
+        hk_scan_a<<<nbT, 256, 0, stream>>>(ncur, Tn, scanpre, scanbs);
+        hk_scan_b<<<1, 256, 0, stream>>>(scanbs, nbT);
+        hk_scan_c<<<(Tn + 255) / 256, 256, 0, stream>>>(scanpre, scanbs, Tn, nbT, offs);
+    }
+
+    hk_scatter3p<<<8 * 208, 256, 0, stream>>>(gg_src, gg_dst, dg_src, dg_dst,
+                                              gd_src, gd_dst, EGG, EDG, EGD,
+                                              NG, offs, rank, csr, 8.0f / (float)Tn);
 
     const int gb = NGp / 64, db = NDp / 64;
-
-    if (tier >= 1) {
-        int* rank = (int*)meanP;
-        hk_count3r<<<(ET + 255) / 256, 256, 0, stream>>>(gg_dst, dg_dst, gd_dst,
-                                                         EGG, EDG, EGD, NG, ncur, rank, bnbuf);
-        {
-            int nbT = (Tn + 2047) / 2048;
-            hk_scan_a<<<nbT, 256, 0, stream>>>(ncur, Tn, scanpre, scanbs);
-            hk_scan_b<<<1, 256, 0, stream>>>(scanbs, nbT);
-            hk_scan_c<<<(Tn + 255) / 256, 256, 0, stream>>>(scanpre, scanbs, Tn, nbT, offs, ncur);
-        }
-        hk_scatter3p<<<8 * 208, 256, 0, stream>>>(gg_src, gg_dst, dg_src, dg_dst,
-                                                  gd_src, gd_dst, EGG, EDG, EGD,
-                                                  NG, offs, rank, csr, 8.0f / (float)Tn);
+    unsigned* xg16u = (unsigned*)xg16;
+    unsigned* xd16u = (unsigned*)xd16;
+    unsigned* hg0u = (unsigned*)hg0;
+    unsigned* hd0u = (unsigned*)hd0;
+    const float* bnG = bnbuf + 512;
+    const float* bnD = bnbuf + 768;
+
+    FS G = {}, D = {};
+
+    G.gsrc[0] = xg16u; G.goffs[0] = offs;          G.gbn[0] = 0;
+    G.gsrc[1] = xd16u; G.goffs[1] = offs + NG;     G.gbn[1] = 0;
+    G.ssrc = xg16u; G.sbn = 0; G.csr = csr;
+    G.W[0] = wf0n;            G.W[1] = wf0n + 2048;
+    G.W[2] = wf0n + 2 * 4096; G.W[3] = wf0n + 2 * 4096 + 2048;
+    G.W[4] = wf0sum;          G.W[5] = wf0sum + 2048;
+    G.bb = b0; G.b1off = 0; G.b2off = 256;
+    G.N = NG; G.out = hg0; G.stats = bnbuf;
+    D.gsrc[0] = xg16u; D.goffs[0] = offs + 2 * NG; D.gbn[0] = 0;
+    D.ssrc = xd16u; D.sbn = 0; D.csr = csr;
+    D.W[0] = wf0n + 4096; D.W[1] = wf0n + 4096 + 2048;
+    D.W[2] = wf0s + 4096; D.W[3] = wf0s + 4096 + 2048;
+    D.bb = b0; D.b1off = 128; D.b2off = -1;
+    D.N = ND; D.out = hd0; D.stats = bnbuf + 256;
+    hk_fsage<2, 1, 2, 32, 36, false><<<gb + db, 512, 0, stream>>>(G, D, gb, dflag);
+    hk_bnfinal2<<<1, 256, 0, stream>>>(bnbuf, 1.f / NG, 1.f / ND, bng, 0L, 128L, bnb, 0L, 128L, dflag);
+
+    G = FS{}; D = FS{};
+    G.gsrc[0] = hg0u; G.goffs[0] = offs;          G.gbn[0] = bnG;
+    G.gsrc[1] = hd0u; G.goffs[1] = offs + NG;     G.gbn[1] = bnD;
+    G.ssrc = hg0u; G.sbn = bnG; G.csr = csr;
+    for (int ks = 0; ks < 4; ks++) {
+        G.W[ks] = wf1n + ks * 2048;
+        G.W[4 + ks] = wf1n + 2 * 8192 + ks * 2048;
+        G.W[8 + ks] = wf1sum + ks * 2048;
+        D.W[ks] = wf1n + 8192 + ks * 2048;
+        D.W[4 + ks] = wf1s + 8192 + ks * 2048;
+    }
+    G.bb = b1; G.b1off = 0; G.b2off = 256;
+    G.N = NG; G.out = pg1; G.stats = bnbuf;
+    D.gsrc[0] = hg0u; D.goffs[0] = offs + 2 * NG; D.gbn[0] = bnG;
+    D.ssrc = hd0u; D.sbn = bnD; D.csr = csr;
+    D.bb = b1; D.b1off = 128; D.b2off = -1;
+    D.N = ND; D.out = pd1; D.stats = bnbuf + 256;
+    hk_fsage<2, 1, 4, 64, 68, true><<<gb + db, 512, 0, stream>>>(G, D, gb, dflag);
+    hk_bnfinal2<<<1, 256, 0, stream>>>(bnbuf, 1.f / NG, 1.f / ND, bng, 256L, 384L, bnb, 256L, 384L, dflag);
+
+    if (tier == 2) {
+        hk_proj2<<<gb + db, 256, 0, stream>>>(pg1, NG, pd1, ND, gb, Wp, bp,
+                                              outf, outf + (long)NG * 64, bnbuf, dflag);
     } else {
-        hk_count3<<<(ET + 255) / 256, 256, 0, stream>>>(gg_dst, dg_dst, gd_dst,
-                                                        EGG, EDG, EGD, NG, ncur);
-        {
-            int nbT = (Tn + 2047) / 2048;
-            hk_scan_a<<<nbT, 256, 0, stream>>>(ncur, Tn, scanpre, scanbs);
-            hk_scan_b<<<1, 256, 0, stream>>>(scanbs, nbT);
-            hk_scan_c<<<(Tn + 255) / 256, 256, 0, stream>>>(scanpre, scanbs, Tn, nbT, offs, ncur);
-        }
-        hk_scatter3<<<(ET + 255) / 256, 256, 0, stream>>>(gg_src, gg_dst, dg_src, dg_dst,
-                                                          gd_src, gd_dst, EGG, EDG, EGD,
-                                                          NG, ncur, csr, bnbuf);
-    }
-
-    if (tier >= 1) {
-        unsigned* xg16u = (unsigned*)xg16;
-        unsigned* xd16u = (unsigned*)xd16;
-        unsigned* hg0u = (unsigned*)hg0;
-        unsigned* hd0u = (unsigned*)hd0;
-        unsigned* mggM = meanP;
-        unsigned* mdg0 = meanP + (long)NGp * 32;
-        unsigned* mdg1 = meanP + (long)NGp * 64;
-        u16* pd1 = (tier == 2) ? pd1ws : pd1out;
-
-        DS3 G = {}, D = {};
-
-        {
-            int nbg = (NG + 15) / 16, nbd = (ND + 15) / 16;
-            hk_mean32a<<<2 * nbg + nbd, 256, 0, stream>>>(xg16u, xd16u, offs, csr,
-                                                          mggM, mdg0, mgdM, NG, ND, nbg);
-        }
-        G.AT[0] = mggM;  G.W[0] = wf0n;             G.W[1] = wf0n + 2048;
-        G.AT[1] = mdg0;  G.W[2] = wf0n + 2 * 4096;  G.W[3] = wf0n + 2 * 4096 + 2048;
-        G.AT[2] = xg16u; G.W[4] = wf0sum;           G.W[5] = wf0sum + 2048;
-        G.bb = b0; G.b1off = 0; G.b2off = 256;
-        G.N = NG; G.out = hg0; G.stats = bnbuf;
-        D.AT[0] = mgdM;  D.W[0] = wf0n + 4096;      D.W[1] = wf0n + 4096 + 2048;
-        D.AT[1] = xd16u; D.W[2] = wf0s + 4096;      D.W[3] = wf0s + 4096 + 2048;
-        D.bb = b0; D.b1off = 128; D.b2off = -1;
-        D.N = ND; D.out = hd0; D.stats = bnbuf + 256;
-        hk_dsage3<3, 2, 2, 32, 36><<<gb + db, 512, 0, stream>>>(G, D, gb, dflag);
-        hk_bnfinal2<<<1, 256, 0, stream>>>(bnbuf, 1.f / NG, 1.f / ND, bng, 0L, 128L, bnb, 0L, 128L, dflag);
-        hk_bnapply2<<<(int)(((long)(NG + ND) * 16 + 255) / 256), 256, 0, stream>>>(
-            hg0, (long)NG * 16, hd0, (long)ND * 16, bnbuf);
-
-        {
-            int nbg = (NG + 7) / 8, nbd = (ND + 7) / 8;
-            hk_mean64a<<<2 * nbg + nbd, 256, 0, stream>>>(hg0u, hd0u, offs, csr,
-                                                          mggM, mdg1, mgdM, NG, ND, nbg);
-        }
-        G = DS3{}; D = DS3{};
-        G.AT[0] = mggM;  G.AT[1] = mdg1;  G.AT[2] = hg0u;
-        D.AT[0] = mgdM;  D.AT[1] = hd0u;
-        for (int ks = 0; ks < 4; ks++) {
-            G.W[ks] = wf1n + ks * 2048;
-            G.W[4 + ks] = wf1n + 2 * 8192 + ks * 2048;
-            G.W[8 + ks] = wf1sum + ks * 2048;
-            D.W[ks] = wf1n + 8192 + ks * 2048;
-            D.W[4 + ks] = wf1s + 8192 + ks * 2048;
-        }
-        G.bb = b1; G.b1off = 0; G.b2off = 256;
-        G.N = NG; G.out = pg1; G.stats = bnbuf;
-        D.bb = b1; D.b1off = 128; D.b2off = -1;
-        D.N = ND; D.out = pd1; D.stats = bnbuf + 256;
-        hk_dsage3<3, 2, 4, 64, 68><<<gb + db, 512, 0, stream>>>(G, D, gb, dflag);
-        hk_bnfinal2<<<1, 256, 0, stream>>>(bnbuf, 1.f / NG, 1.f / ND, bng, 256L, 384L, bnb, 256L, 384L, dflag);
-
-        if (tier == 2) {
-            hk_proj2<<<gb + db, 256, 0, stream>>>(pg1, NG, pd1, ND, gb, Wp, bp,
-                                                  outf, outf + (long)NG * 64, bnbuf, dflag);
-        } else {
-            hk_proj2<<<db, 256, 0, stream>>>(pg1, NG, pd1, ND, 0, Wp, bp,
-                                             outf, outf + (long)NG * 64, bnbuf, dflag);
-            hk_proj2<<<gb, 256, 0, stream>>>(pg1, NG, pd1, ND, gb, Wp, bp,
-                                             outf, outf + (long)NG * 64, bnbuf, dflag);
-        }
-    } else {
-        SageP G, D;
-
-        G.h1 = xg; G.off1 = offs;          G.csr1 = csr;
-        G.h2 = xd; G.off2 = offs + NG;     G.csr2 = csr;
-        G.hs = xg;
-        G.Wf1 = wf0n; G.Wf2 = wf0n + 2 * 4096;
-        G.WfS1 = wf0s; G.WfS2 = wf0s + 2 * 4096;
-        G.bb = b0; G.b1off = 0; G.b2off = 256;
-        G.N = NG; G.out = hg0; G.stats = bnbuf;
-        D.h1 = xg; D.off1 = offs + 2 * NG; D.csr1 = csr;
-        D.h2 = 0; D.off2 = 0; D.csr2 = 0;
-        D.hs = xd;
-        D.Wf1 = wf0n + 4096; D.Wf2 = 0;
-        D.WfS1 = wf0s + 4096; D.WfS2 = 0;
-        D.bb = b0; D.b1off = 128; D.b2off = -1;
-        D.N = ND; D.out = hd0; D.stats = bnbuf + 256;
-        hk_sage64m<<<gb + db, 256, 0, stream>>>(G, D, gb, dflag);
-        hk_bnfinal2<<<1, 256, 0, stream>>>(bnbuf, 1.f / NG, 1.f / ND, bng, 0L, 128L, bnb, 0L, 128L, dflag);
-        hk_bnapply2<<<(int)(((long)(NG + ND) * 16 + 255) / 256), 256, 0, stream>>>(
-            hg0, (long)NG * 16, hd0, (long)ND * 16, bnbuf);
-
-        G.h1 = hg0; G.off1 = offs;          G.csr1 = csr;
-        G.h2 = hd0; G.off2 = offs + NG;     G.csr2 = csr;
-        G.hs = hg0;
-        G.Wf1 = wf1n; G.Wf2 = wf1n + 2 * 8192;
-        G.WfS1 = wf1s; G.WfS2 = wf1s + 2 * 8192;
-        G.bb = b1; G.b1off = 0; G.b2off = 256;
-        G.N = NG; G.out = pg1; G.stats = bnbuf;
-        D.h1 = hg0; D.off1 = offs + 2 * NG; D.csr1 = csr;
-        D.h2 = 0; D.off2 = 0; D.csr2 = 0;
-        D.hs = hd0;
-        D.Wf1 = wf1n + 8192; D.Wf2 = 0;
-        D.WfS1 = wf1s + 8192; D.WfS2 = 0;
-        D.bb = b1; D.b1off = 128; D.b2off = -1;
-        D.N = ND; D.out = pd1out; D.stats = bnbuf + 256;
-        hk_sage128m<<<gb + db, 256, 0, stream>>>(G, D, gb, dflag);
-        hk_bnfinal2<<<1, 256, 0, stream>>>(bnbuf, 1.f / NG, 1.f / ND, bng, 256L, 384L, bnb, 256L, 384L, dflag);
-        hk_bnapply2<<<(int)(((long)(NG + ND) * 16 + 255) / 256), 256, 0, stream>>>(
-            pg1, (long)NG * 16, pd1out, (long)ND * 16, bnbuf);
-
-        hk_proj<<<db, 256, 0, stream>>>(pd1out, ND, Wp, 8192L, bp, 64L, outf + (long)NG * 64, dflag);
-        hk_proj<<<gb, 256, 0, stream>>>(pg1, NG, Wp, 0L, bp, 0L, outf, dflag);
-    }
-}
+        hk_proj2<<<db, 256, 0, stream>>>(pg1, NG, pd1, ND, 0, Wp, bp,
+                                         outf, outf + (long)NG * 64, bnbuf, dflag);
+        hk_proj2<<<gb, 256, 0, stream>>>(pg1, NG, pd1, ND, gb, Wp, bp,
+                                         outf, outf + (long)NG * 64, bnbuf, dflag);
+    }
+}
```

Result: slower. 443.9 us (+4.2%).
